# Optimization experiments

Hardware: AMD Instinct MI355X
Metric: run time of the kernel (lower is better)

The kernel has to match this reference:

```python
import jax, jax.numpy as jnp
import numpy as np

INV_SQRT_2 = float(1.0 / np.sqrt(2.0))
INV_SQRT_3 = float(1.0 / np.sqrt(3.0))


def _silu(x):
    return x * jax.nn.sigmoid(x)


def _residual_stack(x, Ws):
    # Ws: (n_layers, 2, d, d); each layer: two (Dense -> silu), residual add, *1/sqrt(2)
    for l in range(Ws.shape[0]):
        y = x
        for i in range(Ws.shape[1]):
            y = _silu(y @ Ws[l, i])
        x = (x + y) * INV_SQRT_2
    return x


def _eff_bilinear(basis, m, id_reduce, ragged, W, n_edges, kmax):
    # basis: (T, B), m: (T, I), W: (I, B, O). Ragged rows packed into dense (E, Kmax, .)
    b2 = jnp.zeros((n_edges, kmax, basis.shape[1]), basis.dtype).at[id_reduce, ragged].set(basis)
    m2 = jnp.zeros((n_edges, kmax, m.shape[1]), m.dtype).at[id_reduce, ragged].set(m)
    sum_k = jnp.einsum('ekb,eki->ebi', b2, m2)          # (E, B, I)
    return jnp.einsum('ebi,ibo->eo', sum_k, W)          # (E, O)


def setup_inputs() -> dict:
    key = jax.random.key(0)
    N, E, K = 8000, 80000, 6
    T = E * K
    D, DR, DC, DS, DT3, DB, DQ = 128, 16, 16, 16, 64, 64, 64
    ks = jax.random.split(key, 32)
    r = lambda i, shape, s=1.0: jax.random.normal(ks[i], shape, jnp.float32) * s
    w = 0.05
    return dict(
        h=r(0, (N, D)), m_st=r(1, (E, D)),
        rbf_h=jax.random.uniform(ks[2], (E, DR)),
        rbf3=jax.random.uniform(ks[3], (E, DR)),
        cbf3=jax.random.uniform(ks[4], (T, DC)),
        sbf4=jax.random.uniform(ks[5], (T, DS)),
        idx_s=jax.random.randint(ks[6], (E,), 0, N),
        idx_t=jax.random.randint(ks[7], (E,), 0, N),
        idx_swap=jax.random.permutation(ks[8], E),
        id3_kt=jax.random.randint(ks[9], (T,), 0, E),
        id3_st=jnp.repeat(jnp.arange(E), K),
        id3_ragged_idx=jnp.tile(jnp.arange(K), E),
        edge_nb_idx=jnp.repeat(jnp.arange(E), K),
        edge_nb_ragged_idx=jnp.tile(jnp.arange(K), E),
        Kt=K, Kq=K,
        W_skip=r(10, (D, D), w),
        Wt_mkt=r(11, (D, D), w), Wt_rbf=r(12, (DR, D), w), Wt_down=r(13, (D, DT3), w),
        Wt_cbf=r(14, (DT3, DC, DB), w), Wt_up_st=r(15, (DB, D), w), Wt_up_ts=r(16, (DB, D), w),
        Wq_down=r(17, (D, DQ), w), Wq_sbf=r(18, (DQ, DS, DQ), w),
        Wq_up_st=r(19, (DQ, D), w), Wq_up_ts=r(20, (DQ, D), w),
        Wres_before=r(21, (1, 2, D, D), w), Wres_after=r(22, (2, 2, D, D), w),
        Wres_m=r(23, (1, 2, D, D), w),
        W_ae_rbf=r(24, (DR, D), w), W_ae_dense=r(25, (D, D), w), W_ae_res=r(26, (2, 2, D, D), w),
        W_asi=r(27, (3 * D, D), w),
    )


def reference(h, m_st, rbf_h, rbf3, cbf3, sbf4, idx_s, idx_t, idx_swap, id3_kt,
              id3_st, id3_ragged_idx, edge_nb_idx, edge_nb_ragged_idx, Kt, Kq,
              W_skip, Wt_mkt, Wt_rbf, Wt_down, Wt_cbf, Wt_up_st, Wt_up_ts,
              Wq_down, Wq_sbf, Wq_up_st, Wq_up_ts, Wres_before, Wres_after,
              Wres_m, W_ae_rbf, W_ae_dense, W_ae_res, W_asi):
    N, E = h.shape[0], m_st.shape[0]

    x_skip = m_st @ W_skip

    # Quadruplet interaction (ScaleFactor == identity)
    m_d = _silu(m_st @ Wq_down)                       # (E, emb_quad)
    m_nb = m_d[edge_nb_idx]                            # (E_NB, emb_quad)
    xq = _eff_bilinear(sbf4, m_nb, edge_nb_idx, edge_nb_ragged_idx, Wq_sbf, E, Kq)
    x4 = (_silu(xq @ Wq_up_st) + _silu(xq @ Wq_up_ts)[idx_swap]) * INV_SQRT_2

    # Triplet interaction
    m_kt = _silu(m_st @ Wt_mkt)
    m_kt = m_kt * (rbf3 @ Wt_rbf)                      # scale_rbf identity
    m_kt = _silu(m_kt @ Wt_down)                       # (E, emb_triplet)
    m_kt = m_kt[id3_kt]                                # (T, emb_triplet)
    xt = _eff_bilinear(cbf3, m_kt, id3_st, id3_ragged_idx, Wt_cbf, E, Kt)
    x3 = (_silu(xt @ Wt_up_st) + _silu(xt @ Wt_up_ts)[idx_swap]) * INV_SQRT_2

    x = (x_skip + x3 + x4) * INV_SQRT_3
    x = _residual_stack(x, Wres_before)
    m = (m_st + x) * INV_SQRT_2
    m = _residual_stack(m, Wres_after)

    # AtomEmbedding: rbf-gated scatter-add of edge messages to target atoms
    x_ae = m * (rbf_h @ W_ae_rbf)
    h2 = jax.ops.segment_sum(x_ae, idx_t, num_segments=N)   # scale_sum identity
    h2 = _silu(h2 @ W_ae_dense)
    h2 = _residual_stack(h2, W_ae_res)
    h_new = (h + h2) * INV_SQRT_2

    # AtomSelfInteraction
    m2 = _silu(jnp.concatenate([h_new[idx_s], h_new[idx_t], m], axis=-1) @ W_asi)
    m2 = _residual_stack(m2, Wres_m)
    m_out = (m + m2) * INV_SQRT_2
    return h_new, m_out
```

## Files before the change

kernel.cpp:

```cpp
#include <hip/hip_runtime.h>

#define INV_SQRT_2 0.70710678118654752440f
#define INV_SQRT_3 0.57735026918962576451f

typedef __bf16 bf16_t;
typedef __bf16 bf16x8 __attribute__((ext_vector_type(8)));
typedef __bf16 bf16x4 __attribute__((ext_vector_type(4)));
typedef float f32x4 __attribute__((ext_vector_type(4)));

__device__ __forceinline__ float toF(float x) { return x; }
__device__ __forceinline__ float toF(bf16_t x) { return (float)x; }
__device__ __forceinline__ float siluf(float x) { return x / (1.f + __expf(-x)); }

template <typename T> __device__ __forceinline__ T fromF(float x);
template <> __device__ __forceinline__ float fromF<float>(float x) { return x; }
template <> __device__ __forceinline__ bf16_t fromF<bf16_t>(float x) { return (bf16_t)x; }

__device__ __forceinline__ bf16x8 ld8(const bf16_t* p) { return *(const bf16x8*)p; }
__device__ __forceinline__ bf16x8 ld8(const float* p) {
  bf16x8 r;
#pragma unroll
  for (int j = 0; j < 8; ++j) r[j] = (bf16_t)p[j];
  return r;
}

__device__ __forceinline__ f32x4 MFMA(bf16x8 a, bf16x8 b, f32x4 c) {
  return __builtin_amdgcn_mfma_f32_16x16x32_bf16(a, b, c, 0, 0, 0);
}

__device__ __forceinline__ void zero8(f32x4 (&a)[8]) {
#pragma unroll
  for (int i = 0; i < 8; ++i)
#pragma unroll
    for (int q = 0; q < 4; ++q) a[i][q] = 0.f;
}
__device__ __forceinline__ void zero4(f32x4 (&a)[4]) {
#pragma unroll
  for (int i = 0; i < 4; ++i)
#pragma unroll
    for (int q = 0; q < 4; ++q) a[i][q] = 0.f;
}

__device__ __forceinline__ bf16x8 ldB(const bf16_t* Bp, int ks, int nt, int NT, int lane) {
  return *(const bf16x8*)(Bp + ((((size_t)ks * NT + nt) * 64 + lane) << 3));
}

template <bool WS, int SZ>
__device__ __forceinline__ f32x4 mfma2(bf16x8 a, const bf16_t* Bp, int ks, int nt, int NT,
                                       int lane, f32x4 c) {
  c = MFMA(a, ldB(Bp, ks, nt, NT, lane), c);
  if (WS) c = MFMA(a, ldB(Bp + SZ, ks, nt, NT, lane), c);
  return c;
}

template <int NC>
struct StReg { bf16x8 v[NC]; };
template <int NC>
__device__ __forceinline__ void st_issue(StReg<NC>& r, const bf16_t* src, int tid) {
#pragma unroll
  for (int i = 0; i < NC; ++i) r.v[i] = *(const bf16x8*)(src + ((i * 512 + tid) << 3));
}
template <int NC>
__device__ __forceinline__ void st_commit(const StReg<NC>& r, bf16_t* dst, int tid) {
#pragma unroll
  for (int i = 0; i < NC; ++i) *(bf16x8*)&dst[(i * 512 + tid) << 3] = r.v[i];
}

template <int KS, int NT>
__device__ __forceinline__ void pass_glob(f32x4 (&acc)[NT], const bf16x8* af,
                                          const bf16_t* Wbuf, int lane) {
#pragma unroll
  for (int ks = 0; ks < KS; ++ks)
#pragma unroll
    for (int nt = 0; nt < NT; ++nt)
      acc[nt] = MFMA(af[ks], *(const bf16x8*)&Wbuf[((ks * NT + nt) * 64 + lane) << 3], acc[nt]);
}
template <int KS>
__device__ __forceinline__ void pass_slab(f32x4 (&acc)[8], const bf16_t* slab,
                                          const bf16_t* Wbuf, int lane) {
  const int rc = lane & 15, g = lane >> 4;
#pragma unroll
  for (int ks = 0; ks < KS; ++ks) {
    bf16x8 a = *(const bf16x8*)&slab[rc * 136 + ks * 32 + (g << 3)];
#pragma unroll
    for (int nt = 0; nt < 8; ++nt)
      acc[nt] = MFMA(a, *(const bf16x8*)&Wbuf[((ks * 8 + nt) * 64 + lane) << 3], acc[nt]);
  }
}

__global__ void k_detect(const unsigned short* __restrict__ probe, int* __restrict__ flag) {
  __shared__ int cnt;
  if (threadIdx.x == 0) cnt = 0;
  __syncthreads();
  int bad = 0;
  for (int i = threadIdx.x; i < 256; i += 64) {
    unsigned int u = (unsigned int)probe[i] << 16;
    float v = __uint_as_float(u);
    if (!(v == v) || fabsf(v) > 4.f || v < -0.25f) bad++;
  }
  atomicAdd(&cnt, bad);
  __syncthreads();
  if (threadIdx.x == 0) *flag = (cnt > 16) ? 1 : 0;
}

__global__ void k_zero(float* __restrict__ p, int n) {
  int i = blockIdx.x * blockDim.x + threadIdx.x;
  if (i < n) p[i] = 0.f;
}

#define GUARD if (*flag != want) return;

struct RDesc { const void* src; int K, N, Kpad, dstoff, mode; };
struct RTable { RDesc d[25]; };

template <typename TIN>
__global__ void k_repack(const int* __restrict__ flag, int want, RTable tab,
                         bf16_t* __restrict__ out) {
  GUARD
  RDesc d = tab.d[blockIdx.y];
  int p = blockIdx.x * 256 + threadIdx.x;
  int sz = d.Kpad * d.N;
  if (p >= sz) return;
  int NT = d.N >> 4;
  int j = p & 7;
  int lane = (p >> 3) & 63;
  int q = p >> 9;
  int nt = q % NT, ks = q / NT;
  int k = ks * 32 + ((lane >> 4) << 3) + j;
  int col = nt * 16 + (lane & 15);
  size_t si = d.mode ? ((size_t)(k & 63) * 16 + (k >> 6)) * 64 + col
                     : (size_t)k * d.N + col;
  float v = (k < d.K) ? toF(((const TIN*)d.src)[si]) : 0.f;
  bf16_t hi = (bf16_t)v;
  out[d.dstoff + p] = hi;
  out[d.dstoff + sz + p] = (bf16_t)(v - (float)hi);
}

template <typename TIN, bool WS>
__global__ __launch_bounds__(256) void k_bil_mf(const int* __restrict__ flag, int want,
    const TIN* __restrict__ basis, const bf16_t* __restrict__ msrc,
    const int* __restrict__ gidx, const bf16_t* __restrict__ Wc,
    bf16_t* __restrict__ out) {
  GUARD
  __shared__ __align__(16) bf16_t Ms[96 * 72];
  __shared__ __align__(16) float Bas[16 * 100];
  __shared__ __align__(16) bf16_t P[16384];
  const int tid = threadIdx.x;
  const int e0 = blockIdx.x * 16;
#pragma unroll
  for (int it = 0; it < 3; ++it) {
    int c = tid + it * 256;
    int j = c >> 3, part = c & 7;
    int row = gidx[e0 * 6 + j];
    *(bf16x8*)&Ms[j * 72 + part * 8] = ld8(msrc + (size_t)row * 64 + part * 8);
  }
#pragma unroll
  for (int it = 0; it < 6; ++it) {
    int c = tid + it * 256;
    Bas[(c / 96) * 100 + (c % 96)] = toF(basis[(size_t)e0 * 96 + c]);
  }
  __syncthreads();
  {
    const int e = tid >> 4, sub = tid & 15, i0 = sub * 4;
    float acc[16][4];
#pragma unroll
    for (int b = 0; b < 16; ++b)
#pragma unroll
      for (int j = 0; j < 4; ++j) acc[b][j] = 0.f;
#pragma unroll
    for (int k = 0; k < 6; ++k) {
      bf16x4 mv = *(const bf16x4*)&Ms[(e * 6 + k) * 72 + i0];
      float mf[4];
#pragma unroll
      for (int j = 0; j < 4; ++j) mf[j] = (float)mv[j];
      const float* bp = &Bas[e * 100 + k * 16];
#pragma unroll
      for (int b4 = 0; b4 < 4; ++b4) {
        f32x4 bv = *(const f32x4*)&bp[b4 * 4];
#pragma unroll
        for (int bb = 0; bb < 4; ++bb)
#pragma unroll
          for (int j = 0; j < 4; ++j) acc[b4 * 4 + bb][j] += bv[bb] * mf[j];
      }
    }
#pragma unroll
    for (int b = 0; b < 16; ++b) {
      int kk = b * 64 + i0;
      int ks = kk >> 5, r5 = kk & 31;
      int lane_hi = r5 >> 3, jj = r5 & 7;
      bf16x4 w;
#pragma unroll
      for (int j = 0; j < 4; ++j) w[j] = (bf16_t)acc[b][j];
      *(bf16x4*)&P[ks * 512 + lane_hi * 128 + e * 8 + jj] = w;
    }
  }
  __syncthreads();
  const int lane = tid & 63, wid = tid >> 6;
  const int rc = lane & 15, g = lane >> 4;
  f32x4 oa[4];
  zero4(oa);
#pragma unroll
  for (int k4 = 0; k4 < 8; ++k4)
#pragma unroll
    for (int j = 0; j < 4; ++j) {
      int ks = k4 * 4 + j;
      oa[j] = mfma2<WS, 65536>(*(const bf16x8*)&P[ks * 512 + lane * 8], Wc, ks, wid, 4, lane,
                               oa[j]);
    }
  f32x4 oacc = (oa[0] + oa[1]) + (oa[2] + oa[3]);
  bf16_t* op = out + ((size_t)e0 + g * 4) * 64 + wid * 16 + rc;
#pragma unroll
  for (int r = 0; r < 4; ++r) op[(size_t)r * 64] = (bf16_t)oacc[r];
}

template <typename TIN, bool WS>
__global__ __launch_bounds__(512, 2) void k_comb2(const int* __restrict__ flag, int want,
    const TIN* __restrict__ mst, const bf16_t* __restrict__ xt, const bf16_t* __restrict__ xq,
    const int* __restrict__ idx_swap,
    const bf16_t* Wsk, const bf16_t* Wtst, const bf16_t* Wtts,
    const bf16_t* Wqst, const bf16_t* Wqts,
    bf16_t* __restrict__ X, int M) {
  GUARD
  __shared__ __align__(16) bf16_t Wb[2][16384];
  const int tid = threadIdx.x;
  const int lane = tid & 63, wid = tid >> 6;
  const int grow0 = blockIdx.x * 128 + wid * 16;
  const int rc = lane & 15, g = lane >> 4;
  const int arow = grow0 + rc;
  const int srow = idx_swap[arow];

  const bf16_t* wseq[5] = {Wsk, Wtst, Wtts, Wqst, Wqts};
  const int SZs[5] = {16384, 8192, 8192, 8192, 8192};

  StReg<4> sreg;
  st_issue<4>(sreg, wseq[0], tid);
  st_commit<4>(sreg, Wb[0], tid);
  __syncthreads();
  int cur = 0;
  f32x4 total[8];
  f32x4 acc[8];
  zero8(acc);
  bf16x8 af[4];
#pragma unroll
  for (int l = 0; l < 5; ++l) {
    if (l == 0) {
#pragma unroll
      for (int ks = 0; ks < 4; ++ks)
        af[ks] = ld8(mst + (size_t)arow * 128 + ks * 32 + (g << 3));
    } else {
      const bf16_t* asrc = (l <= 2) ? xt : xq;
      int r = (l == 1 || l == 3) ? arow : srow;
#pragma unroll
      for (int ks = 0; ks < 2; ++ks) af[ks] = ld8(asrc + (size_t)r * 64 + ks * 32 + (g << 3));
    }
#pragma unroll
    for (int p = 0; p < (WS ? 2 : 1); ++p) {
      bool last_stage = (l == 4) && (p == (WS ? 1 : 0));
      if (!last_stage) {
        const bf16_t* nx = (WS && p == 0) ? wseq[l] + SZs[l] : wseq[l + 1];
        st_issue<4>(sreg, nx, tid);
      }
      if (l == 0) pass_glob<4, 8>(acc, af, Wb[cur], lane);
      else        pass_glob<2, 8>(acc, af, Wb[cur], lane);
      if (!last_stage) {
        st_commit<4>(sreg, Wb[cur ^ 1], tid);
        __syncthreads();
        cur ^= 1;
      }
    }
    if (l == 0) {
#pragma unroll
      for (int nt = 0; nt < 8; ++nt) total[nt] = acc[nt] * INV_SQRT_3;
    } else {
#pragma unroll
      for (int nt = 0; nt < 8; ++nt)
#pragma unroll
        for (int r = 0; r < 4; ++r)
          total[nt][r] += siluf(acc[nt][r]) * (INV_SQRT_2 * INV_SQRT_3);
    }
    zero8(acc);
  }
  bf16_t* op = X + (size_t)(grow0 + g * 4) * 128 + rc;
#pragma unroll
  for (int nt = 0; nt < 8; ++nt)
#pragma unroll
    for (int r = 0; r < 4; ++r) op[(size_t)r * 128 + nt * 16] = (bf16_t)total[nt][r];
}

template <typename TIN, bool WS>
__global__ __launch_bounds__(512, 1) void k_resE2(const int* __restrict__ flag, int want,
    const bf16_t* __restrict__ Xg, const TIN* __restrict__ mst,
    const bf16_t* W0, const bf16_t* W1, const bf16_t* W2,
    const bf16_t* W3, const bf16_t* W4, const bf16_t* W5,
    bf16_t* __restrict__ outg, int M) {
  GUARD
  __shared__ __align__(16) bf16_t Xs[128 * 136];
  __shared__ __align__(16) bf16_t Ys[128 * 136];
  __shared__ __align__(16) bf16_t Wb[2][16384];
  const int tid = threadIdx.x;
  const int lane = tid & 63, wid = tid >> 6;
  const int grow0 = blockIdx.x * 128 + wid * 16;
  const int rc = lane & 15, g = lane >> 4;
  bf16_t* slabX = Xs + wid * 16 * 136;
  bf16_t* slabY = Ys + wid * 16 * 136;

  const bf16_t* seq[12];
  if (WS) {
    seq[0] = W0; seq[1] = W0 + 16384; seq[2] = W1; seq[3] = W1 + 16384;
    seq[4] = W2; seq[5] = W2 + 16384; seq[6] = W3; seq[7] = W3 + 16384;
    seq[8] = W4; seq[9] = W4 + 16384; seq[10] = W5; seq[11] = W5 + 16384;
  } else {
    seq[0] = W0; seq[1] = W1; seq[2] = W2; seq[3] = W3; seq[4] = W4; seq[5] = W5;
  }
  const int NW = WS ? 12 : 6;

  StReg<4> sreg;
  st_issue<4>(sreg, seq[0], tid);
#pragma unroll
  for (int i = 0; i < 4; ++i) {
    int o = (i * 64 + lane) * 8;
    int r = o >> 7, c = o & 127;
    *(bf16x8*)&slabX[r * 136 + c] = ld8(Xg + (size_t)(grow0 + r) * 128 + c);
  }
  st_commit<4>(sreg, Wb[0], tid);
  __syncthreads();

  f32x4 acc[8];
  zero8(acc);
  int cur = 0;
#pragma unroll
  for (int s = 0; s < NW; ++s) {
    if (s + 1 < NW) st_issue<4>(sreg, seq[s + 1], tid);
    const int gg = WS ? (s >> 1) : s;
    const bool fin = WS ? ((s & 1) != 0) : true;
    pass_slab<4>(acc, (gg & 1) ? slabY : slabX, Wb[cur], lane);
    if (fin) {
      if ((gg & 1) == 0) {
#pragma unroll
        for (int nt = 0; nt < 8; ++nt)
#pragma unroll
          for (int r = 0; r < 4; ++r)
            slabY[(g * 4 + r) * 136 + nt * 16 + rc] = (bf16_t)siluf(acc[nt][r]);
      } else {
#pragma unroll
        for (int nt = 0; nt < 8; ++nt)
#pragma unroll
          for (int r = 0; r < 4; ++r) {
            int ix = (g * 4 + r) * 136 + nt * 16 + rc;
            float v = ((float)slabX[ix] + siluf(acc[nt][r])) * INV_SQRT_2;
            if (gg == 1) {
              float mv = toF(mst[(size_t)(grow0 + g * 4 + r) * 128 + nt * 16 + rc]);
              v = (mv + v) * INV_SQRT_2;
            }
            slabX[ix] = (bf16_t)v;
          }
      }
      zero8(acc);
    }
    if (s + 1 < NW) {
      st_commit<4>(sreg, Wb[cur ^ 1], tid);
      __syncthreads();
      cur ^= 1;
    }
  }
#pragma unroll
  for (int i = 0; i < 4; ++i) {
    int o = (i * 64 + lane) * 8;
    int r = o >> 7, c = o & 127;
    *(bf16x8*)&outg[(size_t)(grow0 + r) * 128 + c] = *(const bf16x8*)&slabX[r * 136 + c];
  }
}

template <bool WS>
__global__ __launch_bounds__(512, 1) void k_resN2(const int* __restrict__ flag, int want,
    bf16_t* __restrict__ Xg, const bf16_t* W0, const bf16_t* W1, const bf16_t* W2,
    const bf16_t* W3, int M) {
  GUARD
  __shared__ __align__(16) bf16_t Xs[128 * 136];
  __shared__ __align__(16) bf16_t Ys[128 * 136];
  __shared__ __align__(16) bf16_t Wb[2][16384];
  const int tid = threadIdx.x;
  const int lane = tid & 63, wid = tid >> 6;
  const int grow0 = blockIdx.x * 128 + wid * 16;
  const bool act = grow0 < M;
  const int rc = lane & 15, g = lane >> 4;
  bf16_t* slabX = Xs + wid * 16 * 136;
  bf16_t* slabY = Ys + wid * 16 * 136;

  const bf16_t* seq[8];
  if (WS) {
    seq[0] = W0; seq[1] = W0 + 16384; seq[2] = W1; seq[3] = W1 + 16384;
    seq[4] = W2; seq[5] = W2 + 16384; seq[6] = W3; seq[7] = W3 + 16384;
  } else {
    seq[0] = W0; seq[1] = W1; seq[2] = W2; seq[3] = W3;
  }
  const int NW = WS ? 8 : 4;

  StReg<4> sreg;
  st_issue<4>(sreg, seq[0], tid);
  if (act) {
#pragma unroll
    for (int i = 0; i < 4; ++i) {
      int o = (i * 64 + lane) * 8;
      int r = o >> 7, c = o & 127;
      *(bf16x8*)&slabX[r * 136 + c] = ld8(Xg + (size_t)(grow0 + r) * 128 + c);
    }
  }
  st_commit<4>(sreg, Wb[0], tid);
  __syncthreads();

  f32x4 acc[8];
  zero8(acc);
  int cur = 0;
#pragma unroll
  for (int s = 0; s < NW; ++s) {
    if (s + 1 < NW) st_issue<4>(sreg, seq[s + 1], tid);
    const int gg = WS ? (s >> 1) : s;
    const bool fin = WS ? ((s & 1) != 0) : true;
    pass_slab<4>(acc, (gg & 1) ? slabY : slabX, Wb[cur], lane);
    if (fin) {
      if ((gg & 1) == 0) {
#pragma unroll
        for (int nt = 0; nt < 8; ++nt)
#pragma unroll
          for (int r = 0; r < 4; ++r)
            slabY[(g * 4 + r) * 136 + nt * 16 + rc] = (bf16_t)siluf(acc[nt][r]);
      } else {
#pragma unroll
        for (int nt = 0; nt < 8; ++nt)
#pragma unroll
          for (int r = 0; r < 4; ++r) {
            int ix = (g * 4 + r) * 136 + nt * 16 + rc;
            slabX[ix] = (bf16_t)(((float)slabX[ix] + siluf(acc[nt][r])) * INV_SQRT_2);
          }
      }
      zero8(acc);
    }
    if (s + 1 < NW) {
      st_commit<4>(sreg, Wb[cur ^ 1], tid);
      __syncthreads();
      cur ^= 1;
    }
  }
  if (act) {
#pragma unroll
    for (int i = 0; i < 4; ++i) {
      int o = (i * 64 + lane) * 8;
      int r = o >> 7, c = o & 127;
      *(bf16x8*)&Xg[(size_t)(grow0 + r) * 128 + c] = *(const bf16x8*)&slabX[r * 136 + c];
    }
  }
}

template <typename TIN, typename TOUT, bool WS>
__global__ __launch_bounds__(512, 1) void k_asi2(const int* __restrict__ flag, int want,
    const bf16_t* __restrict__ hnew, const bf16_t* __restrict__ m,
    const int* __restrict__ idx_s, const int* __restrict__ idx_t,
    const bf16_t* Wasi, const bf16_t* Wm0, const bf16_t* Wm1,
    TOUT* __restrict__ outm, int M) {
  GUARD
  __shared__ __align__(16) bf16_t Xs[128 * 136];
  __shared__ __align__(16) bf16_t Ys[128 * 136];
  __shared__ __align__(16) bf16_t Wb[2][16384];
  const int tid = threadIdx.x;
  const int lane = tid & 63, wid = tid >> 6;
  const int grow0 = blockIdx.x * 128 + wid * 16;
  const int rc = lane & 15, g = lane >> 4;
  bf16_t* slabX = Xs + wid * 16 * 136;
  bf16_t* slabY = Ys + wid * 16 * 136;
  const int e = grow0 + rc;
  const int rs = idx_s[e], rt = idx_t[e];

  const bf16_t* seq[10];
  if (WS) {
    seq[0] = Wasi;         seq[1] = Wasi + 49152;
    seq[2] = Wasi + 16384; seq[3] = Wasi + 65536;
    seq[4] = Wasi + 32768; seq[5] = Wasi + 81920;
    seq[6] = Wm0;          seq[7] = Wm0 + 16384;
    seq[8] = Wm1;          seq[9] = Wm1 + 16384;
  } else {
    seq[0] = Wasi; seq[1] = Wasi + 16384; seq[2] = Wasi + 32768;
    seq[3] = Wm0;  seq[4] = Wm1;
  }
  const int NW = WS ? 10 : 5;

  StReg<4> sreg;
  st_issue<4>(sreg, seq[0], tid);
  st_commit<4>(sreg, Wb[0], tid);
  __syncthreads();

  f32x4 acc[8];
  zero8(acc);
  bf16x8 af[4];
  int cur = 0;
#pragma unroll
  for (int s = 0; s < NW; ++s) {
    if (s + 1 < NW) st_issue<4>(sreg, seq[s + 1], tid);
    const int lg = WS ? (s >> 1) : s;
    const bool first = WS ? ((s & 1) == 0) : true;
    const bool fin = WS ? ((s & 1) != 0) : true;
    if (lg <= 2) {
      if (first) {
        const bf16_t* asrc = (lg == 0) ? hnew + (size_t)rs * 128
                           : (lg == 1) ? hnew + (size_t)rt * 128
                                       : m + (size_t)e * 128;
#pragma unroll
        for (int ks = 0; ks < 4; ++ks) af[ks] = ld8(asrc + ks * 32 + (g << 3));
      }
      pass_glob<4, 8>(acc, af, Wb[cur], lane);
    } else if (lg == 3) {
      pass_slab<4>(acc, slabX, Wb[cur], lane);
    } else {
      pass_slab<4>(acc, slabY, Wb[cur], lane);
    }
    if (fin) {
      if (lg == 2) {
#pragma unroll
        for (int nt = 0; nt < 8; ++nt)
#pragma unroll
          for (int r = 0; r < 4; ++r)
            slabX[(g * 4 + r) * 136 + nt * 16 + rc] = (bf16_t)siluf(acc[nt][r]);
        zero8(acc);
      } else if (lg == 3) {
#pragma unroll
        for (int nt = 0; nt < 8; ++nt)
#pragma unroll
          for (int r = 0; r < 4; ++r)
            slabY[(g * 4 + r) * 136 + nt * 16 + rc] = (bf16_t)siluf(acc[nt][r]);
        zero8(acc);
      } else if (lg == 4) {
#pragma unroll
        for (int nt = 0; nt < 8; ++nt)
#pragma unroll
          for (int r = 0; r < 4; ++r) {
            int row = grow0 + g * 4 + r, col = nt * 16 + rc;
            float x = (float)slabX[(g * 4 + r) * 136 + col];
            float v = (x + siluf(acc[nt][r])) * INV_SQRT_2;
            outm[(size_t)row * 128 + col] =
                fromF<TOUT>(((float)m[(size_t)row * 128 + col] + v) * INV_SQRT_2);
          }
      }
    }
    if (s + 1 < NW) {
      st_commit<4>(sreg, Wb[cur ^ 1], tid);
      __syncthreads();
      cur ^= 1;
    }
  }
}

template <typename TIN, bool WS>
__global__ __launch_bounds__(512, 2) void k_mkt2(const int* __restrict__ flag, int want,
    const TIN* __restrict__ mst, const TIN* __restrict__ rbf3,
    const bf16_t* __restrict__ Wm, const bf16_t* __restrict__ Wr,
    bf16_t* __restrict__ out, int M) {
  GUARD
  __shared__ __align__(16) bf16_t Wb[2][16384];
  __shared__ __align__(16) bf16_t Wrl[8192];
  const int tid = threadIdx.x;
  const int lane = tid & 63, wid = tid >> 6;
  const int grow0 = blockIdx.x * 128 + wid * 16;
  const int rc = lane & 15, g = lane >> 4;
  StReg<4> sreg;
  st_issue<4>(sreg, Wm, tid);
  bf16x8 wr0 = *(const bf16x8*)(Wr + (tid << 3));
  bf16x8 wr1 = *(const bf16x8*)(Wr + 4096 + (tid << 3));
  st_commit<4>(sreg, Wb[0], tid);
  *(bf16x8*)&Wrl[tid << 3] = wr0;
  *(bf16x8*)&Wrl[4096 + (tid << 3)] = wr1;
  __syncthreads();
  bf16x8 af[4];
#pragma unroll
  for (int ks = 0; ks < 4; ++ks)
    af[ks] = ld8(mst + (size_t)(grow0 + rc) * 128 + ks * 32 + (g << 3));
  bf16x8 az;
#pragma unroll
  for (int j = 0; j < 8; ++j) az[j] = (bf16_t)0.f;
  if (g < 2) az = ld8(rbf3 + (size_t)(grow0 + rc) * 16 + (g << 3));
  f32x4 ag[8];
  zero8(ag);
#pragma unroll
  for (int nt = 0; nt < 8; ++nt) {
    ag[nt] = MFMA(az, *(const bf16x8*)&Wrl[(nt * 64 + lane) << 3], ag[nt]);
    if (WS) ag[nt] = MFMA(az, *(const bf16x8*)&Wrl[4096 + ((nt * 64 + lane) << 3)], ag[nt]);
  }
  f32x4 am[8];
  zero8(am);
  if (WS) st_issue<4>(sreg, Wm + 16384, tid);
  pass_glob<4, 8>(am, af, Wb[0], lane);
  if (WS) {
    st_commit<4>(sreg, Wb[1], tid);
    __syncthreads();
    pass_glob<4, 8>(am, af, Wb[1], lane);
  }
  bf16_t* op = out + (size_t)(grow0 + g * 4) * 128 + rc;
#pragma unroll
  for (int nt = 0; nt < 8; ++nt)
#pragma unroll
    for (int r = 0; r < 4; ++r)
      op[(size_t)r * 128 + nt * 16] = (bf16_t)(siluf(am[nt][r]) * ag[nt][r]);
}

template <typename TA, bool WS>
__global__ __launch_bounds__(512, 2) void k_gemmE2(const int* __restrict__ flag, int want,
    const TA* __restrict__ A, const bf16_t* __restrict__ W, bf16_t* __restrict__ out, int M) {
  GUARD
  __shared__ __align__(16) bf16_t Wb[2][8192];
  const int tid = threadIdx.x;
  const int lane = tid & 63, wid = tid >> 6;
  const int grow0 = blockIdx.x * 128 + wid * 16;
  const int rc = lane & 15, g = lane >> 4;
  StReg<2> sreg;
  st_issue<2>(sreg, W, tid);
  st_commit<2>(sreg, Wb[0], tid);
  __syncthreads();
  bf16x8 af[4];
#pragma unroll
  for (int ks = 0; ks < 4; ++ks)
    af[ks] = ld8(A + (size_t)(grow0 + rc) * 128 + ks * 32 + (g << 3));
  f32x4 acc[4];
  zero4(acc);
  if (WS) st_issue<2>(sreg, W + 8192, tid);
  pass_glob<4, 4>(acc, af, Wb[0], lane);
  if (WS) {
    st_commit<2>(sreg, Wb[1], tid);
    __syncthreads();
    pass_glob<4, 4>(acc, af, Wb[1], lane);
  }
  bf16_t* op = out + (size_t)(grow0 + g * 4) * 64 + rc;
#pragma unroll
  for (int nt = 0; nt < 4; ++nt)
#pragma unroll
    for (int r = 0; r < 4; ++r) op[(size_t)r * 64 + nt * 16] = (bf16_t)siluf(acc[nt][r]);
}

template <bool WS>
__global__ __launch_bounds__(512, 2) void k_gemmN2(const int* __restrict__ flag, int want,
    const float* __restrict__ A, const bf16_t* __restrict__ W, bf16_t* __restrict__ out, int M) {
  GUARD
  __shared__ __align__(16) bf16_t Wb[2][16384];
  const int tid = threadIdx.x;
  const int lane = tid & 63, wid = tid >> 6;
  const int grow0 = blockIdx.x * 128 + wid * 16;
  const bool act = grow0 < M;
  const int rc = lane & 15, g = lane >> 4;
  StReg<4> sreg;
  st_issue<4>(sreg, W, tid);
  st_commit<4>(sreg, Wb[0], tid);
  __syncthreads();
  bf16x8 af[4];
  if (act) {
#pragma unroll
    for (int ks = 0; ks < 4; ++ks)
      af[ks] = ld8(A + (size_t)(grow0 + rc) * 128 + ks * 32 + (g << 3));
  } else {
#pragma unroll
    for (int ks = 0; ks < 4; ++ks)
#pragma unroll
      for (int j = 0; j < 8; ++j) af[ks][j] = (bf16_t)0.f;
  }
  f32x4 acc[8];
  zero8(acc);
  if (WS) st_issue<4>(sreg, W + 16384, tid);
  pass_glob<4, 8>(acc, af, Wb[0], lane);
  if (WS) {
    st_commit<4>(sreg, Wb[1], tid);
    __syncthreads();
    pass_glob<4, 8>(acc, af, Wb[1], lane);
  }
  if (act) {
    bf16_t* op = out + (size_t)(grow0 + g * 4) * 128 + rc;
#pragma unroll
    for (int nt = 0; nt < 8; ++nt)
#pragma unroll
      for (int r = 0; r < 4; ++r) op[(size_t)r * 128 + nt * 16] = (bf16_t)siluf(acc[nt][r]);
  }
}

template <typename TIN>
__global__ void k_scatter(const int* __restrict__ flag, int want,
                          const bf16_t* __restrict__ m, const TIN* __restrict__ rbf_h,
                          const TIN* __restrict__ Wrbf, const int* __restrict__ idx_t,
                          float* __restrict__ h2) {
  GUARD
  int e = blockIdx.x;
  int c = threadIdx.x;
  float g = 0.f;
#pragma unroll
  for (int k = 0; k < 16; ++k) g += toF(rbf_h[(size_t)e * 16 + k]) * toF(Wrbf[k * 128 + c]);
  atomicAdd(&h2[(size_t)idx_t[e] * 128 + c], (float)m[(size_t)e * 128 + c] * g);
}

template <typename TIN, typename TOUT>
__global__ void k_hnew_b(const int* __restrict__ flag, int want,
                         const TIN* __restrict__ h, bf16_t* __restrict__ X,
                         TOUT* __restrict__ out, int n) {
  GUARD
  int i = blockIdx.x * blockDim.x + threadIdx.x;
  if (i >= n) return;
  float v = (toF(h[i]) + (float)X[i]) * INV_SQRT_2;
  X[i] = (bf16_t)v;
  out[i] = fromF<TOUT>(v);
}

template <typename TIN, typename TOUT, bool WS>
static void run_pipeline(void* const* d_in, int N, int E, void* d_out,
                         bf16_t* Wpack, bf16_t* s0, bf16_t* s1, bf16_t* s2, bf16_t* s3,
                         float* h2, bf16_t* Rn2, const int* flag, int want, hipStream_t stream) {
  const TIN* h      = (const TIN*)d_in[0];
  const TIN* m_st   = (const TIN*)d_in[1];
  const TIN* rbf_h  = (const TIN*)d_in[2];
  const TIN* rbf3   = (const TIN*)d_in[3];
  const TIN* cbf3   = (const TIN*)d_in[4];
  const TIN* sbf4   = (const TIN*)d_in[5];
  const int* idx_s   = (const int*)d_in[6];
  const int* idx_t   = (const int*)d_in[7];
  const int* idx_sw  = (const int*)d_in[8];
  const int* id3_kt  = (const int*)d_in[9];
  const int* enb_idx = (const int*)d_in[12];
  const TIN* W_skip   = (const TIN*)d_in[16];
  const TIN* Wt_mkt   = (const TIN*)d_in[17];
  const TIN* Wt_rbf   = (const TIN*)d_in[18];
  const TIN* Wt_down  = (const TIN*)d_in[19];
  const TIN* Wt_cbf   = (const TIN*)d_in[20];
  const TIN* Wt_up_st = (const TIN*)d_in[21];
  const TIN* Wt_up_ts = (const TIN*)d_in[22];
  const TIN* Wq_down  = (const TIN*)d_in[23];
  const TIN* Wq_sbf   = (const TIN*)d_in[24];
  const TIN* Wq_up_st = (const TIN*)d_in[25];
  const TIN* Wq_up_ts = (const TIN*)d_in[26];
  const TIN* Wres_before = (const TIN*)d_in[27];
  const TIN* Wres_after  = (const TIN*)d_in[28];
  const TIN* Wres_m      = (const TIN*)d_in[29];
  const TIN* W_ae_rbf    = (const TIN*)d_in[30];
  const TIN* W_ae_dense  = (const TIN*)d_in[31];
  const TIN* W_ae_res    = (const TIN*)d_in[32];
  const TIN* W_asi       = (const TIN*)d_in[33];

  RTable tab;
  int cur = 0, nd = 0;
  auto add = [&](const void* src, int K, int Np, int Kpad, int mode = 0) {
    tab.d[nd].src = src; tab.d[nd].K = K; tab.d[nd].N = Np; tab.d[nd].Kpad = Kpad;
    tab.d[nd].dstoff = cur; tab.d[nd].mode = mode;
    int o = cur;
    cur += 2 * Kpad * Np;
    ++nd;
    return o;
  };
  const int M128 = 128 * 128;
  int oQd  = add(Wq_down, 128, 64, 128);
  int oMkt = add(Wt_mkt, 128, 128, 128);
  int oRbf = add(Wt_rbf, 16, 128, 32);
  int oTd  = add(Wt_down, 128, 64, 128);
  int oTst = add(Wt_up_st, 64, 128, 64);
  int oTts = add(Wt_up_ts, 64, 128, 64);
  int oQst = add(Wq_up_st, 64, 128, 64);
  int oQts = add(Wq_up_ts, 64, 128, 64);
  int oSk  = add(W_skip, 128, 128, 128);
  int oB0  = add(Wres_before, 128, 128, 128);
  int oB1  = add(Wres_before + M128, 128, 128, 128);
  int oA0  = add(Wres_after, 128, 128, 128);
  int oA1  = add(Wres_after + M128, 128, 128, 128);
  int oA2  = add(Wres_after + 2 * M128, 128, 128, 128);
  int oA3  = add(Wres_after + 3 * M128, 128, 128, 128);
  int oM0  = add(Wres_m, 128, 128, 128);
  int oM1  = add(Wres_m + M128, 128, 128, 128);
  int oAed = add(W_ae_dense, 128, 128, 128);
  int oAe0 = add(W_ae_res, 128, 128, 128);
  int oAe1 = add(W_ae_res + M128, 128, 128, 128);
  int oAe2 = add(W_ae_res + 2 * M128, 128, 128, 128);
  int oAe3 = add(W_ae_res + 3 * M128, 128, 128, 128);
  int oAsi = add(W_asi, 384, 128, 384);
  int oTc  = add(Wt_cbf, 1024, 64, 1024, 1);
  int oQc  = add(Wq_sbf, 1024, 64, 1024, 1);
  (void)cur;

  const int gE = E / 128;
  const int gN = (N + 127) / 128;
  const int BS = 256;

  bf16_t* mkt_tmp = s0;
  bf16_t* m_kt = s2;
  bf16_t* m_d  = s3;
  bf16_t* xt = s0;
  bf16_t* xq = s1;
  bf16_t* X  = s2;
  bf16_t* R2 = s0;

  k_repack<TIN><<<dim3(256, 25), BS, 0, stream>>>(flag, want, tab, Wpack);

  k_mkt2<TIN, WS><<<gE, 512, 0, stream>>>(flag, want, m_st, rbf3, Wpack + oMkt, Wpack + oRbf,
                                          mkt_tmp, E);
  k_gemmE2<bf16_t, WS><<<gE, 512, 0, stream>>>(flag, want, mkt_tmp, Wpack + oTd, m_kt, E);
  k_gemmE2<TIN, WS><<<gE, 512, 0, stream>>>(flag, want, m_st, Wpack + oQd, m_d, E);
  k_bil_mf<TIN, WS><<<E / 16, BS, 0, stream>>>(flag, want, cbf3, m_kt, id3_kt, Wpack + oTc, xt);
  k_bil_mf<TIN, WS><<<E / 16, BS, 0, stream>>>(flag, want, sbf4, m_d, enb_idx, Wpack + oQc, xq);
  k_comb2<TIN, WS><<<gE, 512, 0, stream>>>(flag, want, m_st, xt, xq, idx_sw,
      Wpack + oSk, Wpack + oTst, Wpack + oTts, Wpack + oQst, Wpack + oQts, X, E);
  k_resE2<TIN, WS><<<gE, 512, 0, stream>>>(flag, want, X, m_st, Wpack + oB0, Wpack + oB1,
      Wpack + oA0, Wpack + oA1, Wpack + oA2, Wpack + oA3, R2, E);
  k_zero<<<(N * 128 + BS - 1) / BS, BS, 0, stream>>>(h2, N * 128);
  k_scatter<TIN><<<E, 128, 0, stream>>>(flag, want, R2, rbf_h, W_ae_rbf, idx_t, h2);
  k_gemmN2<WS><<<gN, 512, 0, stream>>>(flag, want, h2, Wpack + oAed, Rn2, N);
  k_resN2<WS><<<gN, 512, 0, stream>>>(flag, want, Rn2, Wpack + oAe0, Wpack + oAe1,
                                      Wpack + oAe2, Wpack + oAe3, N);
  TOUT* out_h = (TOUT*)d_out;
  TOUT* out_m = out_h + (size_t)N * 128;
  k_hnew_b<TIN, TOUT><<<(N * 128 + BS - 1) / BS, BS, 0, stream>>>(flag, want, h, Rn2, out_h,
                                                                  N * 128);
  k_asi2<TIN, TOUT, WS><<<gE, 512, 0, stream>>>(flag, want, Rn2, R2, idx_s, idx_t,
      Wpack + oAsi, Wpack + oM0, Wpack + oM1, out_m, E);
}

extern "C" void kernel_launch(void* const* d_in, const int* in_sizes, int n_in,
                              void* d_out, int out_size, void* d_ws, size_t ws_size,
                              hipStream_t stream) {
  const int D = 128;
  const int N = in_sizes[0] / D;
  const int E = in_sizes[1] / D;

  char* base = (char*)d_ws;
  bf16_t* Wpack = (bf16_t*)base;
  int* flag = (int*)(base + 1916928 + 32768);
  char* dyn = base + 1916928 + 32768 + 256;
  size_t U = (size_t)E * 64 * sizeof(bf16_t);
  bf16_t* s0 = (bf16_t*)dyn;
  bf16_t* s1 = (bf16_t*)(dyn + U);
  bf16_t* s2 = (bf16_t*)(dyn + 2 * U);
  bf16_t* s3 = (bf16_t*)(dyn + 3 * U);
  float* h2 = (float*)(dyn + 2 * U);
  bf16_t* Rn2 = (bf16_t*)((char*)h2 + (size_t)N * 128 * sizeof(float));

  k_detect<<<1, 64, 0, stream>>>((const unsigned short*)d_in[2], flag);

  run_pipeline<bf16_t, bf16_t, false>(d_in, N, E, d_out, Wpack, s0, s1, s2, s3, h2, Rn2, flag, 0,
                                      stream);
  run_pipeline<float, float, true>(d_in, N, E, d_out, Wpack, s0, s1, s2, s3, h2, Rn2, flag, 1,
                                   stream);
}
```

Measured before the change: 669.3 us.

## Merge dtype-specialized pipelines into one runtime-dispatched pipeline with smaller blocks

Replaces the two templated pipelines (bf16 and f32, each launched and early-exiting on a device flag) with a single set of kernels that read the dtype flag at runtime and branch internally. This halves the number of kernel launches. It also shrinks the GEMM kernels from 512-thread, 128-row tiles to 256-thread, 64-row tiles with higher occupancy bounds. The residual kernel now uses a single weight buffer with an extra barrier per stage. The cost is runtime branching, possible register pressure from the merged paths, and less weight reuse per block.

After: 741.5 us. 1.11x slower.

```diff
diff --git a/kernel.cpp b/kernel.cpp
--- a/kernel.cpp
+++ b/kernel.cpp
@@ -12,10 +12,6 @@
 __device__ __forceinline__ float toF(bf16_t x) { return (float)x; }
 __device__ __forceinline__ float siluf(float x) { return x / (1.f + __expf(-x)); }
 
-template <typename T> __device__ __forceinline__ T fromF(float x);
-template <> __device__ __forceinline__ float fromF<float>(float x) { return x; }
-template <> __device__ __forceinline__ bf16_t fromF<bf16_t>(float x) { return (bf16_t)x; }
-
 __device__ __forceinline__ bf16x8 ld8(const bf16_t* p) { return *(const bf16x8*)p; }
 __device__ __forceinline__ bf16x8 ld8(const float* p) {
   bf16x8 r;
@@ -24,6 +20,10 @@
   return r;
 }
 
+__device__ __forceinline__ float ldsc(const void* p, int f32, size_t i) {
+  return f32 ? ((const float*)p)[i] : toF(((const bf16_t*)p)[i]);
+}
+
 __device__ __forceinline__ f32x4 MFMA(bf16x8 a, bf16x8 b, f32x4 c) {
   return __builtin_amdgcn_mfma_f32_16x16x32_bf16(a, b, c, 0, 0, 0);
 }
@@ -45,25 +45,35 @@
   return *(const bf16x8*)(Bp + ((((size_t)ks * NT + nt) * 64 + lane) << 3));
 }
 
-template <bool WS, int SZ>
-__device__ __forceinline__ f32x4 mfma2(bf16x8 a, const bf16_t* Bp, int ks, int nt, int NT,
-                                       int lane, f32x4 c) {
-  c = MFMA(a, ldB(Bp, ks, nt, NT, lane), c);
-  if (WS) c = MFMA(a, ldB(Bp + SZ, ks, nt, NT, lane), c);
-  return c;
-}
-
-template <int NC>
-struct StReg { bf16x8 v[NC]; };
-template <int NC>
-__device__ __forceinline__ void st_issue(StReg<NC>& r, const bf16_t* src, int tid) {
-#pragma unroll
-  for (int i = 0; i < NC; ++i) r.v[i] = *(const bf16x8*)(src + ((i * 512 + tid) << 3));
-}
-template <int NC>
-__device__ __forceinline__ void st_commit(const StReg<NC>& r, bf16_t* dst, int tid) {
-#pragma unroll
-  for (int i = 0; i < NC; ++i) *(bf16x8*)&dst[(i * 512 + tid) << 3] = r.v[i];
+__device__ __forceinline__ void ldA(bf16x8 (&af)[4], const void* p, int f32, size_t row, int g) {
+  if (f32) {
+    const float* q = (const float*)p + row * 128 + (g << 3);
+#pragma unroll
+    for (int ks = 0; ks < 4; ++ks) af[ks] = ld8(q + ks * 32);
+  } else {
+    const bf16_t* q = (const bf16_t*)p + row * 128 + (g << 3);
+#pragma unroll
+    for (int ks = 0; ks < 4; ++ks) af[ks] = ld8(q + ks * 32);
+  }
+}
+
+struct St8 { bf16x8 v[8]; };
+__device__ __forceinline__ void issue8(St8& r, const bf16_t* src, int tid) {
+#pragma unroll
+  for (int i = 0; i < 8; ++i) r.v[i] = *(const bf16x8*)(src + ((i * 256 + tid) << 3));
+}
+__device__ __forceinline__ void commit8(const St8& r, bf16_t* dst, int tid) {
+#pragma unroll
+  for (int i = 0; i < 8; ++i) *(bf16x8*)&dst[(i * 256 + tid) << 3] = r.v[i];
+}
+struct St4 { bf16x8 v[4]; };
+__device__ __forceinline__ void issue4(St4& r, const bf16_t* src, int tid) {
+#pragma unroll
+  for (int i = 0; i < 4; ++i) r.v[i] = *(const bf16x8*)(src + ((i * 256 + tid) << 3));
+}
+__device__ __forceinline__ void commit4(const St4& r, bf16_t* dst, int tid) {
+#pragma unroll
+  for (int i = 0; i < 4; ++i) *(bf16x8*)&dst[(i * 256 + tid) << 3] = r.v[i];
 }
 
 template <int KS, int NT>
@@ -108,19 +118,17 @@
   if (i < n) p[i] = 0.f;
 }
 
-#define GUARD if (*flag != want) return;
-
 struct RDesc { const void* src; int K, N, Kpad, dstoff, mode; };
 struct RTable { RDesc d[25]; };
 
-template <typename TIN>
-__global__ void k_repack(const int* __restrict__ flag, int want, RTable tab,
-                         bf16_t* __restrict__ out) {
-  GUARD
+__global__ void k_repack(const int* __restrict__ flag, RTable tab, bf16_t* __restrict__ out) {
+  const int ws = *flag;
   RDesc d = tab.d[blockIdx.y];
   int p = blockIdx.x * 256 + threadIdx.x;
   int sz = d.Kpad * d.N;
   if (p >= sz) return;
+  const int bilin = d.mode & 1;
+  const int Koff = d.mode >> 1;
   int NT = d.N >> 4;
   int j = p & 7;
   int lane = (p >> 3) & 63;
@@ -128,20 +136,19 @@
   int nt = q % NT, ks = q / NT;
   int k = ks * 32 + ((lane >> 4) << 3) + j;
   int col = nt * 16 + (lane & 15);
-  size_t si = d.mode ? ((size_t)(k & 63) * 16 + (k >> 6)) * 64 + col
-                     : (size_t)k * d.N + col;
-  float v = (k < d.K) ? toF(((const TIN*)d.src)[si]) : 0.f;
+  size_t si = bilin ? ((size_t)(k & 63) * 16 + (k >> 6)) * 64 + col
+                    : (size_t)(k + Koff) * d.N + col;
+  float v = (k < d.K) ? ldsc(d.src, ws, si) : 0.f;
   bf16_t hi = (bf16_t)v;
   out[d.dstoff + p] = hi;
   out[d.dstoff + sz + p] = (bf16_t)(v - (float)hi);
 }
 
-template <typename TIN, bool WS>
-__global__ __launch_bounds__(256) void k_bil_mf(const int* __restrict__ flag, int want,
-    const TIN* __restrict__ basis, const bf16_t* __restrict__ msrc,
+__global__ __launch_bounds__(256) void k_bil(const int* __restrict__ flag,
+    const void* __restrict__ basis, const bf16_t* __restrict__ msrc,
     const int* __restrict__ gidx, const bf16_t* __restrict__ Wc,
     bf16_t* __restrict__ out) {
-  GUARD
+  const int ws = *flag;
   __shared__ __align__(16) bf16_t Ms[96 * 72];
   __shared__ __align__(16) float Bas[16 * 100];
   __shared__ __align__(16) bf16_t P[16384];
@@ -157,7 +164,7 @@
 #pragma unroll
   for (int it = 0; it < 6; ++it) {
     int c = tid + it * 256;
-    Bas[(c / 96) * 100 + (c % 96)] = toF(basis[(size_t)e0 * 96 + c]);
+    Bas[(c / 96) * 100 + (c % 96)] = ldsc(basis, ws, (size_t)e0 * 96 + c);
   }
   __syncthreads();
   {
@@ -199,71 +206,190 @@
   const int rc = lane & 15, g = lane >> 4;
   f32x4 oa[4];
   zero4(oa);
-#pragma unroll
-  for (int k4 = 0; k4 < 8; ++k4)
-#pragma unroll
-    for (int j = 0; j < 4; ++j) {
-      int ks = k4 * 4 + j;
-      oa[j] = mfma2<WS, 65536>(*(const bf16x8*)&P[ks * 512 + lane * 8], Wc, ks, wid, 4, lane,
-                               oa[j]);
-    }
+  if (ws) {
+#pragma unroll
+    for (int k4 = 0; k4 < 8; ++k4)
+#pragma unroll
+      for (int j = 0; j < 4; ++j) {
+        int ks = k4 * 4 + j;
+        bf16x8 a = *(const bf16x8*)&P[ks * 512 + lane * 8];
+        oa[j] = MFMA(a, ldB(Wc, ks, wid, 4, lane), oa[j]);
+        oa[j] = MFMA(a, ldB(Wc + 65536, ks, wid, 4, lane), oa[j]);
+      }
+  } else {
+#pragma unroll
+    for (int k4 = 0; k4 < 8; ++k4)
+#pragma unroll
+      for (int j = 0; j < 4; ++j) {
+        int ks = k4 * 4 + j;
+        bf16x8 a = *(const bf16x8*)&P[ks * 512 + lane * 8];
+        oa[j] = MFMA(a, ldB(Wc, ks, wid, 4, lane), oa[j]);
+      }
+  }
   f32x4 oacc = (oa[0] + oa[1]) + (oa[2] + oa[3]);
   bf16_t* op = out + ((size_t)e0 + g * 4) * 64 + wid * 16 + rc;
 #pragma unroll
   for (int r = 0; r < 4; ++r) op[(size_t)r * 64] = (bf16_t)oacc[r];
 }
 
-template <typename TIN, bool WS>
-__global__ __launch_bounds__(512, 2) void k_comb2(const int* __restrict__ flag, int want,
-    const TIN* __restrict__ mst, const bf16_t* __restrict__ xt, const bf16_t* __restrict__ xq,
-    const int* __restrict__ idx_swap,
-    const bf16_t* Wsk, const bf16_t* Wtst, const bf16_t* Wtts,
-    const bf16_t* Wqst, const bf16_t* Wqts,
-    bf16_t* __restrict__ X, int M) {
-  GUARD
+__global__ __launch_bounds__(256, 2) void k_mkt2(const int* __restrict__ flag,
+    const void* __restrict__ mst, const void* __restrict__ rbf3,
+    const bf16_t* __restrict__ Wm, const bf16_t* __restrict__ Wr,
+    bf16_t* __restrict__ out) {
+  const int ws = *flag;
+  __shared__ __align__(16) bf16_t Wb[2][16384];
+  __shared__ __align__(16) bf16_t Wrl[8192];
+  const int tid = threadIdx.x;
+  const int lane = tid & 63, wid = tid >> 6;
+  const int grow0 = blockIdx.x * 64 + wid * 16;
+  const int rc = lane & 15, g = lane >> 4;
+  St8 s8;
+  issue8(s8, Wm, tid);
+  bf16x8 wr[4];
+#pragma unroll
+  for (int i = 0; i < 4; ++i) wr[i] = *(const bf16x8*)(Wr + ((i * 256 + tid) << 3));
+  commit8(s8, Wb[0], tid);
+#pragma unroll
+  for (int i = 0; i < 4; ++i) *(bf16x8*)&Wrl[(i * 256 + tid) << 3] = wr[i];
+  __syncthreads();
+  bf16x8 af[4];
+  ldA(af, mst, ws, (size_t)(grow0 + rc), g);
+  bf16x8 az;
+#pragma unroll
+  for (int j = 0; j < 8; ++j) az[j] = (bf16_t)0.f;
+  if (g < 2) {
+    if (ws) az = ld8((const float*)rbf3 + (size_t)(grow0 + rc) * 16 + (g << 3));
+    else    az = ld8((const bf16_t*)rbf3 + (size_t)(grow0 + rc) * 16 + (g << 3));
+  }
+  f32x4 ag[8];
+  zero8(ag);
+#pragma unroll
+  for (int nt = 0; nt < 8; ++nt) {
+    ag[nt] = MFMA(az, *(const bf16x8*)&Wrl[(nt * 64 + lane) << 3], ag[nt]);
+    if (ws) ag[nt] = MFMA(az, *(const bf16x8*)&Wrl[4096 + ((nt * 64 + lane) << 3)], ag[nt]);
+  }
+  f32x4 am[8];
+  zero8(am);
+  if (ws) issue8(s8, Wm + 16384, tid);
+  pass_glob<4, 8>(am, af, Wb[0], lane);
+  if (ws) {
+    commit8(s8, Wb[1], tid);
+    __syncthreads();
+    pass_glob<4, 8>(am, af, Wb[1], lane);
+  }
+  bf16_t* op = out + (size_t)(grow0 + g * 4) * 128 + rc;
+#pragma unroll
+  for (int nt = 0; nt < 8; ++nt)
+#pragma unroll
+    for (int r = 0; r < 4; ++r)
+      op[(size_t)r * 128 + nt * 16] = (bf16_t)(siluf(am[nt][r]) * ag[nt][r]);
+}
+
+__global__ __launch_bounds__(256, 4) void k_gemmE2(const int* __restrict__ flag, int a_rt,
+    const void* __restrict__ A, const bf16_t* __restrict__ W, bf16_t* __restrict__ out) {
+  const int ws = *flag;
+  const int af32 = a_rt & ws;
+  __shared__ __align__(16) bf16_t Wb[2][8192];
+  const int tid = threadIdx.x;
+  const int lane = tid & 63, wid = tid >> 6;
+  const int grow0 = blockIdx.x * 64 + wid * 16;
+  const int rc = lane & 15, g = lane >> 4;
+  St4 s4;
+  issue4(s4, W, tid);
+  commit4(s4, Wb[0], tid);
+  __syncthreads();
+  bf16x8 af[4];
+  ldA(af, A, af32, (size_t)(grow0 + rc), g);
+  f32x4 acc[4];
+  zero4(acc);
+  if (ws) issue4(s4, W + 8192, tid);
+  pass_glob<4, 4>(acc, af, Wb[0], lane);
+  if (ws) {
+    commit4(s4, Wb[1], tid);
+    __syncthreads();
+    pass_glob<4, 4>(acc, af, Wb[1], lane);
+  }
+  bf16_t* op = out + (size_t)(grow0 + g * 4) * 64 + rc;
+#pragma unroll
+  for (int nt = 0; nt < 4; ++nt)
+#pragma unroll
+    for (int r = 0; r < 4; ++r) op[(size_t)r * 64 + nt * 16] = (bf16_t)siluf(acc[nt][r]);
+}
+
+__global__ __launch_bounds__(256, 2) void k_gemmN2(const int* __restrict__ flag,
+    const float* __restrict__ A, const bf16_t* __restrict__ W, bf16_t* __restrict__ out) {
+  const int ws = *flag;
   __shared__ __align__(16) bf16_t Wb[2][16384];
   const int tid = threadIdx.x;
   const int lane = tid & 63, wid = tid >> 6;
-  const int grow0 = blockIdx.x * 128 + wid * 16;
+  const int grow0 = blockIdx.x * 64 + wid * 16;
+  const int rc = lane & 15, g = lane >> 4;
+  St8 s8;
+  issue8(s8, W, tid);
+  commit8(s8, Wb[0], tid);
+  __syncthreads();
+  bf16x8 af[4];
+  {
+    const float* q = A + (size_t)(grow0 + rc) * 128 + (g << 3);
+#pragma unroll
+    for (int ks = 0; ks < 4; ++ks) af[ks] = ld8(q + ks * 32);
+  }
+  f32x4 acc[8];
+  zero8(acc);
+  if (ws) issue8(s8, W + 16384, tid);
+  pass_glob<4, 8>(acc, af, Wb[0], lane);
+  if (ws) {
+    commit8(s8, Wb[1], tid);
+    __syncthreads();
+    pass_glob<4, 8>(acc, af, Wb[1], lane);
+  }
+  bf16_t* op = out + (size_t)(grow0 + g * 4) * 128 + rc;
+#pragma unroll
+  for (int nt = 0; nt < 8; ++nt)
+#pragma unroll
+    for (int r = 0; r < 4; ++r) op[(size_t)r * 128 + nt * 16] = (bf16_t)siluf(acc[nt][r]);
+}
+
+__global__ __launch_bounds__(256, 2) void k_comb2(const int* __restrict__ flag,
+    const void* __restrict__ mst, const bf16_t* __restrict__ xt,
+    const bf16_t* __restrict__ xq, const int* __restrict__ idx_swap,
+    const bf16_t* Wsk, const bf16_t* Wtst, const bf16_t* Wtts,
+    const bf16_t* Wqst, const bf16_t* Wqts, bf16_t* __restrict__ X) {
+  const int ws = *flag;
+  __shared__ __align__(16) bf16_t Wb[2][16384];
+  const int tid = threadIdx.x;
+  const int lane = tid & 63, wid = tid >> 6;
+  const int grow0 = blockIdx.x * 64 + wid * 16;
   const int rc = lane & 15, g = lane >> 4;
   const int arow = grow0 + rc;
   const int srow = idx_swap[arow];
-
   const bf16_t* wseq[5] = {Wsk, Wtst, Wtts, Wqst, Wqts};
   const int SZs[5] = {16384, 8192, 8192, 8192, 8192};
-
-  StReg<4> sreg;
-  st_issue<4>(sreg, wseq[0], tid);
-  st_commit<4>(sreg, Wb[0], tid);
+  St8 s8;
+  issue8(s8, wseq[0], tid);
+  commit8(s8, Wb[0], tid);
   __syncthreads();
   int cur = 0;
-  f32x4 total[8];
-  f32x4 acc[8];
+  const int NP = ws ? 2 : 1;
+  f32x4 total[8], acc[8];
   zero8(acc);
   bf16x8 af[4];
-#pragma unroll
   for (int l = 0; l < 5; ++l) {
     if (l == 0) {
-#pragma unroll
-      for (int ks = 0; ks < 4; ++ks)
-        af[ks] = ld8(mst + (size_t)arow * 128 + ks * 32 + (g << 3));
+      ldA(af, mst, ws, (size_t)arow, g);
     } else {
       const bf16_t* asrc = (l <= 2) ? xt : xq;
       int r = (l == 1 || l == 3) ? arow : srow;
-#pragma unroll
-      for (int ks = 0; ks < 2; ++ks) af[ks] = ld8(asrc + (size_t)r * 64 + ks * 32 + (g << 3));
-    }
-#pragma unroll
-    for (int p = 0; p < (WS ? 2 : 1); ++p) {
-      bool last_stage = (l == 4) && (p == (WS ? 1 : 0));
-      if (!last_stage) {
-        const bf16_t* nx = (WS && p == 0) ? wseq[l] + SZs[l] : wseq[l + 1];
-        st_issue<4>(sreg, nx, tid);
-      }
+      af[0] = ld8(asrc + (size_t)r * 64 + (g << 3));
+      af[1] = ld8(asrc + (size_t)r * 64 + 32 + (g << 3));
+    }
+    for (int p = 0; p < NP; ++p) {
+      const bool last = (l == 4) && (p == NP - 1);
+      if (!last) issue8(s8, (ws && p == 0) ? wseq[l] + SZs[l] : wseq[l + 1], tid);
       if (l == 0) pass_glob<4, 8>(acc, af, Wb[cur], lane);
       else        pass_glob<2, 8>(acc, af, Wb[cur], lane);
-      if (!last_stage) {
-        st_commit<4>(sreg, Wb[cur ^ 1], tid);
+      if (!last) {
+        commit8(s8, Wb[cur ^ 1], tid);
         __syncthreads();
         cur ^= 1;
       }
@@ -287,53 +413,51 @@
     for (int r = 0; r < 4; ++r) op[(size_t)r * 128 + nt * 16] = (bf16_t)total[nt][r];
 }
 
-template <typename TIN, bool WS>
-__global__ __launch_bounds__(512, 1) void k_resE2(const int* __restrict__ flag, int want,
-    const bf16_t* __restrict__ Xg, const TIN* __restrict__ mst,
+__global__ __launch_bounds__(256, 2) void k_resE2(const int* __restrict__ flag,
+    const bf16_t* __restrict__ Xg, const void* __restrict__ mst,
     const bf16_t* W0, const bf16_t* W1, const bf16_t* W2,
     const bf16_t* W3, const bf16_t* W4, const bf16_t* W5,
-    bf16_t* __restrict__ outg, int M) {
-  GUARD
-  __shared__ __align__(16) bf16_t Xs[128 * 136];
-  __shared__ __align__(16) bf16_t Ys[128 * 136];
-  __shared__ __align__(16) bf16_t Wb[2][16384];
+    bf16_t* __restrict__ outg) {
+  const int ws = *flag;
+  __shared__ __align__(16) bf16_t Xs[64 * 136];
+  __shared__ __align__(16) bf16_t Ys[64 * 136];
+  __shared__ __align__(16) bf16_t Wb[16384];
   const int tid = threadIdx.x;
   const int lane = tid & 63, wid = tid >> 6;
-  const int grow0 = blockIdx.x * 128 + wid * 16;
-  const int rc = lane & 15, g = lane >> 4;
-  bf16_t* slabX = Xs + wid * 16 * 136;
-  bf16_t* slabY = Ys + wid * 16 * 136;
-
+  const int grow0 = blockIdx.x * 64 + wid * 16;
+  const int rc = lane & 15, g = lane >> 4;
+  bf16_t* slabX = Xs + wid * (16 * 136);
+  bf16_t* slabY = Ys + wid * (16 * 136);
+  const bf16_t* Wl[6] = {W0, W1, W2, W3, W4, W5};
   const bf16_t* seq[12];
-  if (WS) {
-    seq[0] = W0; seq[1] = W0 + 16384; seq[2] = W1; seq[3] = W1 + 16384;
-    seq[4] = W2; seq[5] = W2 + 16384; seq[6] = W3; seq[7] = W3 + 16384;
-    seq[8] = W4; seq[9] = W4 + 16384; seq[10] = W5; seq[11] = W5 + 16384;
+  int NW;
+  if (ws) {
+    NW = 12;
+#pragma unroll
+    for (int l = 0; l < 6; ++l) { seq[2 * l] = Wl[l]; seq[2 * l + 1] = Wl[l] + 16384; }
   } else {
-    seq[0] = W0; seq[1] = W1; seq[2] = W2; seq[3] = W3; seq[4] = W4; seq[5] = W5;
-  }
-  const int NW = WS ? 12 : 6;
-
-  StReg<4> sreg;
-  st_issue<4>(sreg, seq[0], tid);
+    NW = 6;
+#pragma unroll
+    for (int l = 0; l < 6; ++l) seq[l] = Wl[l];
+  }
+  St8 s8;
+  issue8(s8, seq[0], tid);
 #pragma unroll
   for (int i = 0; i < 4; ++i) {
-    int o = (i * 64 + lane) * 8;
-    int r = o >> 7, c = o & 127;
-    *(bf16x8*)&slabX[r * 136 + c] = ld8(Xg + (size_t)(grow0 + r) * 128 + c);
-  }
-  st_commit<4>(sreg, Wb[0], tid);
-  __syncthreads();
-
+    int o = (i * 64 + lane) * 8, r = o >> 7, c = o & 127;
+    *(bf16x8*)&slabX[r * 136 + c] = *(const bf16x8*)&Xg[(size_t)(grow0 + r) * 128 + c];
+  }
+  commit8(s8, Wb, tid);
+  __syncthreads();
   f32x4 acc[8];
   zero8(acc);
-  int cur = 0;
-#pragma unroll
   for (int s = 0; s < NW; ++s) {
-    if (s + 1 < NW) st_issue<4>(sreg, seq[s + 1], tid);
-    const int gg = WS ? (s >> 1) : s;
-    const bool fin = WS ? ((s & 1) != 0) : true;
-    pass_slab<4>(acc, (gg & 1) ? slabY : slabX, Wb[cur], lane);
+    if (s + 1 < NW) issue8(s8, seq[s + 1], tid);
+    const int gg = ws ? (s >> 1) : s;
+    const int fin = ws ? (s & 1) : 1;
+    pass_slab<4>(acc, (gg & 1) ? slabY : slabX, Wb, lane);
+    __syncthreads();
+    if (s + 1 < NW) commit8(s8, Wb, tid);
     if (fin) {
       if ((gg & 1) == 0) {
 #pragma unroll
@@ -348,76 +472,66 @@
           for (int r = 0; r < 4; ++r) {
             int ix = (g * 4 + r) * 136 + nt * 16 + rc;
             float v = ((float)slabX[ix] + siluf(acc[nt][r])) * INV_SQRT_2;
-            if (gg == 1) {
-              float mv = toF(mst[(size_t)(grow0 + g * 4 + r) * 128 + nt * 16 + rc]);
-              v = (mv + v) * INV_SQRT_2;
-            }
+            if (gg == 1)
+              v = (ldsc(mst, ws, (size_t)(grow0 + g * 4 + r) * 128 + nt * 16 + rc) + v) *
+                  INV_SQRT_2;
             slabX[ix] = (bf16_t)v;
           }
       }
       zero8(acc);
     }
-    if (s + 1 < NW) {
-      st_commit<4>(sreg, Wb[cur ^ 1], tid);
-      __syncthreads();
-      cur ^= 1;
-    }
+    if (s + 1 < NW) __syncthreads();
   }
 #pragma unroll
   for (int i = 0; i < 4; ++i) {
-    int o = (i * 64 + lane) * 8;
-    int r = o >> 7, c = o & 127;
+    int o = (i * 64 + lane) * 8, r = o >> 7, c = o & 127;
     *(bf16x8*)&outg[(size_t)(grow0 + r) * 128 + c] = *(const bf16x8*)&slabX[r * 136 + c];
   }
 }
 
-template <bool WS>
-__global__ __launch_bounds__(512, 1) void k_resN2(const int* __restrict__ flag, int want,
-    bf16_t* __restrict__ Xg, const bf16_t* W0, const bf16_t* W1, const bf16_t* W2,
-    const bf16_t* W3, int M) {
-  GUARD
-  __shared__ __align__(16) bf16_t Xs[128 * 136];
-  __shared__ __align__(16) bf16_t Ys[128 * 136];
-  __shared__ __align__(16) bf16_t Wb[2][16384];
+__global__ __launch_bounds__(256, 2) void k_resN2(const int* __restrict__ flag,
+    bf16_t* __restrict__ Xg, const bf16_t* W0, const bf16_t* W1,
+    const bf16_t* W2, const bf16_t* W3) {
+  const int ws = *flag;
+  __shared__ __align__(16) bf16_t Xs[64 * 136];
+  __shared__ __align__(16) bf16_t Ys[64 * 136];
+  __shared__ __align__(16) bf16_t Wb[16384];
   const int tid = threadIdx.x;
   const int lane = tid & 63, wid = tid >> 6;
-  const int grow0 = blockIdx.x * 128 + wid * 16;
-  const bool act = grow0 < M;
-  const int rc = lane & 15, g = lane >> 4;
-  bf16_t* slabX = Xs + wid * 16 * 136;
-  bf16_t* slabY = Ys + wid * 16 * 136;
-
+  const int grow0 = blockIdx.x * 64 + wid * 16;
+  const int rc = lane & 15, g = lane >> 4;
+  bf16_t* slabX = Xs + wid * (16 * 136);
+  bf16_t* slabY = Ys + wid * (16 * 136);
+  const bf16_t* Wl[4] = {W0, W1, W2, W3};
   const bf16_t* seq[8];
-  if (WS) {
-    seq[0] = W0; seq[1] = W0 + 16384; seq[2] = W1; seq[3] = W1 + 16384;
-    seq[4] = W2; seq[5] = W2 + 16384; seq[6] = W3; seq[7] = W3 + 16384;
+  int NW;
+  if (ws) {
+    NW = 8;
+#pragma unroll
+    for (int l = 0; l < 4; ++l) { seq[2 * l] = Wl[l]; seq[2 * l + 1] = Wl[l] + 16384; }
   } else {
-    seq[0] = W0; seq[1] = W1; seq[2] = W2; seq[3] = W3;
-  }
-  const int NW = WS ? 8 : 4;
-
-  StReg<4> sreg;
-  st_issue<4>(sreg, seq[0], tid);
-  if (act) {
-#pragma unroll
-    for (int i = 0; i < 4; ++i) {
-      int o = (i * 64 + lane) * 8;
-      int r = o >> 7, c = o & 127;
-      *(bf16x8*)&slabX[r * 136 + c] = ld8(Xg + (size_t)(grow0 + r) * 128 + c);
-    }
-  }
-  st_commit<4>(sreg, Wb[0], tid);
-  __syncthreads();
-
+    NW = 4;
+#pragma unroll
+    for (int l = 0; l < 4; ++l) seq[l] = Wl[l];
+  }
+  St8 s8;
+  issue8(s8, seq[0], tid);
+#pragma unroll
+  for (int i = 0; i < 4; ++i) {
+    int o = (i * 64 + lane) * 8, r = o >> 7, c = o & 127;
+    *(bf16x8*)&slabX[r * 136 + c] = *(const bf16x8*)&Xg[(size_t)(grow0 + r) * 128 + c];
+  }
+  commit8(s8, Wb, tid);
+  __syncthreads();
   f32x4 acc[8];
   zero8(acc);
-  int cur = 0;
-#pragma unroll
   for (int s = 0; s < NW; ++s) {
-    if (s + 1 < NW) st_issue<4>(sreg, seq[s + 1], tid);
-    const int gg = WS ? (s >> 1) : s;
-    const bool fin = WS ? ((s & 1) != 0) : true;
-    pass_slab<4>(acc, (gg & 1) ? slabY : slabX, Wb[cur], lane);
+    if (s + 1 < NW) issue8(s8, seq[s + 1], tid);
+    const int gg = ws ? (s >> 1) : s;
+    const int fin = ws ? (s & 1) : 1;
+    pass_slab<4>(acc, (gg & 1) ? slabY : slabX, Wb, lane);
+    __syncthreads();
+    if (s + 1 < NW) commit8(s8, Wb, tid);
     if (fin) {
       if ((gg & 1) == 0) {
 #pragma unroll
@@ -436,69 +550,58 @@
       }
       zero8(acc);
     }
-    if (s + 1 < NW) {
-      st_commit<4>(sreg, Wb[cur ^ 1], tid);
-      __syncthreads();
-      cur ^= 1;
-    }
-  }
-  if (act) {
-#pragma unroll
-    for (int i = 0; i < 4; ++i) {
-      int o = (i * 64 + lane) * 8;
-      int r = o >> 7, c = o & 127;
-      *(bf16x8*)&Xg[(size_t)(grow0 + r) * 128 + c] = *(const bf16x8*)&slabX[r * 136 + c];
-    }
-  }
-}
-
-template <typename TIN, typename TOUT, bool WS>
-__global__ __launch_bounds__(512, 1) void k_asi2(const int* __restrict__ flag, int want,
+    if (s + 1 < NW) __syncthreads();
+  }
+#pragma unroll
+  for (int i = 0; i < 4; ++i) {
+    int o = (i * 64 + lane) * 8, r = o >> 7, c = o & 127;
+    *(bf16x8*)&Xg[(size_t)(grow0 + r) * 128 + c] = *(const bf16x8*)&slabX[r * 136 + c];
+  }
+}
+
+__global__ __launch_bounds__(256, 2) void k_asi2(const int* __restrict__ flag,
     const bf16_t* __restrict__ hnew, const bf16_t* __restrict__ m,
     const int* __restrict__ idx_s, const int* __restrict__ idx_t,
     const bf16_t* Wasi, const bf16_t* Wm0, const bf16_t* Wm1,
-    TOUT* __restrict__ outm, int M) {
-  GUARD
-  __shared__ __align__(16) bf16_t Xs[128 * 136];
-  __shared__ __align__(16) bf16_t Ys[128 * 136];
-  __shared__ __align__(16) bf16_t Wb[2][16384];
+    void* __restrict__ outm, int eoff) {
+  const int ws = *flag;
+  __shared__ __align__(16) bf16_t Xs[64 * 136];
+  __shared__ __align__(16) bf16_t Ys[64 * 136];
+  __shared__ __align__(16) bf16_t Wb[16384];
   const int tid = threadIdx.x;
   const int lane = tid & 63, wid = tid >> 6;
-  const int grow0 = blockIdx.x * 128 + wid * 16;
-  const int rc = lane & 15, g = lane >> 4;
-  bf16_t* slabX = Xs + wid * 16 * 136;
-  bf16_t* slabY = Ys + wid * 16 * 136;
+  const int grow0 = blockIdx.x * 64 + wid * 16;
+  const int rc = lane & 15, g = lane >> 4;
+  bf16_t* slabX = Xs + wid * (16 * 136);
+  bf16_t* slabY = Ys + wid * (16 * 136);
   const int e = grow0 + rc;
   const int rs = idx_s[e], rt = idx_t[e];
-
   const bf16_t* seq[10];
-  if (WS) {
+  int NW;
+  if (ws) {
+    NW = 10;
     seq[0] = Wasi;         seq[1] = Wasi + 49152;
     seq[2] = Wasi + 16384; seq[3] = Wasi + 65536;
     seq[4] = Wasi + 32768; seq[5] = Wasi + 81920;
     seq[6] = Wm0;          seq[7] = Wm0 + 16384;
     seq[8] = Wm1;          seq[9] = Wm1 + 16384;
   } else {
+    NW = 5;
     seq[0] = Wasi; seq[1] = Wasi + 16384; seq[2] = Wasi + 32768;
     seq[3] = Wm0;  seq[4] = Wm1;
   }
-  const int NW = WS ? 10 : 5;
-
-  StReg<4> sreg;
-  st_issue<4>(sreg, seq[0], tid);
-  st_commit<4>(sreg, Wb[0], tid);
-  __syncthreads();
-
+  St8 s8;
+  issue8(s8, seq[0], tid);
+  commit8(s8, Wb, tid);
+  __syncthreads();
   f32x4 acc[8];
   zero8(acc);
   bf16x8 af[4];
-  int cur = 0;
-#pragma unroll
   for (int s = 0; s < NW; ++s) {
-    if (s + 1 < NW) st_issue<4>(sreg, seq[s + 1], tid);
-    const int lg = WS ? (s >> 1) : s;
-    const bool first = WS ? ((s & 1) == 0) : true;
-    const bool fin = WS ? ((s & 1) != 0) : true;
+    if (s + 1 < NW) issue8(s8, seq[s + 1], tid);
+    const int lg = ws ? (s >> 1) : s;
+    const int first = ws ? !(s & 1) : 1;
+    const int fin = ws ? (s & 1) : 1;
     if (lg <= 2) {
       if (first) {
         const bf16_t* asrc = (lg == 0) ? hnew + (size_t)rs * 128
@@ -507,12 +610,14 @@
 #pragma unroll
         for (int ks = 0; ks < 4; ++ks) af[ks] = ld8(asrc + ks * 32 + (g << 3));
       }
-      pass_glob<4, 8>(acc, af, Wb[cur], lane);
+      pass_glob<4, 8>(acc, af, Wb, lane);
     } else if (lg == 3) {
-      pass_slab<4>(acc, slabX, Wb[cur], lane);
+      pass_slab<4>(acc, slabX, Wb, lane);
     } else {
-      pass_slab<4>(acc, slabY, Wb[cur], lane);
-    }
+      pass_slab<4>(acc, slabY, Wb, lane);
+    }
+    __syncthreads();
+    if (s + 1 < NW) commit8(s8, Wb, tid);
     if (fin) {
       if (lg == 2) {
 #pragma unroll
@@ -536,280 +641,47 @@
             int row = grow0 + g * 4 + r, col = nt * 16 + rc;
             float x = (float)slabX[(g * 4 + r) * 136 + col];
             float v = (x + siluf(acc[nt][r])) * INV_SQRT_2;
-            outm[(size_t)row * 128 + col] =
-                fromF<TOUT>(((float)m[(size_t)row * 128 + col] + v) * INV_SQRT_2);
+            float res = (toF(m[(size_t)row * 128 + col]) + v) * INV_SQRT_2;
+            size_t oi = (size_t)eoff + (size_t)row * 128 + col;
+            if (ws) ((float*)outm)[oi] = res;
+            else    ((bf16_t*)outm)[oi] = (bf16_t)res;
           }
       }
     }
-    if (s + 1 < NW) {
-      st_commit<4>(sreg, Wb[cur ^ 1], tid);
-      __syncthreads();
-      cur ^= 1;
-    }
-  }
-}
-
-template <typename TIN, bool WS>
-__global__ __launch_bounds__(512, 2) void k_mkt2(const int* __restrict__ flag, int want,
-    const TIN* __restrict__ mst, const TIN* __restrict__ rbf3,
-    const bf16_t* __restrict__ Wm, const bf16_t* __restrict__ Wr,
-    bf16_t* __restrict__ out, int M) {
-  GUARD
-  __shared__ __align__(16) bf16_t Wb[2][16384];
-  __shared__ __align__(16) bf16_t Wrl[8192];
-  const int tid = threadIdx.x;
-  const int lane = tid & 63, wid = tid >> 6;
-  const int grow0 = blockIdx.x * 128 + wid * 16;
-  const int rc = lane & 15, g = lane >> 4;
-  StReg<4> sreg;
-  st_issue<4>(sreg, Wm, tid);
-  bf16x8 wr0 = *(const bf16x8*)(Wr + (tid << 3));
-  bf16x8 wr1 = *(const bf16x8*)(Wr + 4096 + (tid << 3));
-  st_commit<4>(sreg, Wb[0], tid);
-  *(bf16x8*)&Wrl[tid << 3] = wr0;
-  *(bf16x8*)&Wrl[4096 + (tid << 3)] = wr1;
-  __syncthreads();
-  bf16x8 af[4];
-#pragma unroll
-  for (int ks = 0; ks < 4; ++ks)
-    af[ks] = ld8(mst + (size_t)(grow0 + rc) * 128 + ks * 32 + (g << 3));
-  bf16x8 az;
-#pragma unroll
-  for (int j = 0; j < 8; ++j) az[j] = (bf16_t)0.f;
-  if (g < 2) az = ld8(rbf3 + (size_t)(grow0 + rc) * 16 + (g << 3));
-  f32x4 ag[8];
-  zero8(ag);
-#pragma unroll
-  for (int nt = 0; nt < 8; ++nt) {
-    ag[nt] = MFMA(az, *(const bf16x8*)&Wrl[(nt * 64 + lane) << 3], ag[nt]);
-    if (WS) ag[nt] = MFMA(az, *(const bf16x8*)&Wrl[4096 + ((nt * 64 + lane) << 3)], ag[nt]);
-  }
-  f32x4 am[8];
-  zero8(am);
-  if (WS) st_issue<4>(sreg, Wm + 16384, tid);
-  pass_glob<4, 8>(am, af, Wb[0], lane);
-  if (WS) {
-    st_commit<4>(sreg, Wb[1], tid);
-    __syncthreads();
-    pass_glob<4, 8>(am, af, Wb[1], lane);
-  }
-  bf16_t* op = out + (size_t)(grow0 + g * 4) * 128 + rc;
-#pragma unroll
-  for (int nt = 0; nt < 8; ++nt)
-#pragma unroll
-    for (int r = 0; r < 4; ++r)
-      op[(size_t)r * 128 + nt * 16] = (bf16_t)(siluf(am[nt][r]) * ag[nt][r]);
-}
-
-template <typename TA, bool WS>
-__global__ __launch_bounds__(512, 2) void k_gemmE2(const int* __restrict__ flag, int want,
-    const TA* __restrict__ A, const bf16_t* __restrict__ W, bf16_t* __restrict__ out, int M) {
-  GUARD
-  __shared__ __align__(16) bf16_t Wb[2][8192];
-  const int tid = threadIdx.x;
-  const int lane = tid & 63, wid = tid >> 6;
-  const int grow0 = blockIdx.x * 128 + wid * 16;
-  const int rc = lane & 15, g = lane >> 4;
-  StReg<2> sreg;
-  st_issue<2>(sreg, W, tid);
-  st_commit<2>(sreg, Wb[0], tid);
-  __syncthreads();
-  bf16x8 af[4];
-#pragma unroll
-  for (int ks = 0; ks < 4; ++ks)
-    af[ks] = ld8(A + (size_t)(grow0 + rc) * 128 + ks * 32 + (g << 3));
-  f32x4 acc[4];
-  zero4(acc);
-  if (WS) st_issue<2>(sreg, W + 8192, tid);
-  pass_glob<4, 4>(acc, af, Wb[0], lane);
-  if (WS) {
-    st_commit<2>(sreg, Wb[1], tid);
-    __syncthreads();
-    pass_glob<4, 4>(acc, af, Wb[1], lane);
-  }
-  bf16_t* op = out + (size_t)(grow0 + g * 4) * 64 + rc;
-#pragma unroll
-  for (int nt = 0; nt < 4; ++nt)
-#pragma unroll
-    for (int r = 0; r < 4; ++r) op[(size_t)r * 64 + nt * 16] = (bf16_t)siluf(acc[nt][r]);
-}
-
-template <bool WS>
-__global__ __launch_bounds__(512, 2) void k_gemmN2(const int* __restrict__ flag, int want,
-    const float* __restrict__ A, const bf16_t* __restrict__ W, bf16_t* __restrict__ out, int M) {
-  GUARD
-  __shared__ __align__(16) bf16_t Wb[2][16384];
-  const int tid = threadIdx.x;
-  const int lane = tid & 63, wid = tid >> 6;
-  const int grow0 = blockIdx.x * 128 + wid * 16;
-  const bool act = grow0 < M;
-  const int rc = lane & 15, g = lane >> 4;
-  StReg<4> sreg;
-  st_issue<4>(sreg, W, tid);
-  st_commit<4>(sreg, Wb[0], tid);
-  __syncthreads();
-  bf16x8 af[4];
-  if (act) {
-#pragma unroll
-    for (int ks = 0; ks < 4; ++ks)
-      af[ks] = ld8(A + (size_t)(grow0 + rc) * 128 + ks * 32 + (g << 3));
-  } else {
-#pragma unroll
-    for (int ks = 0; ks < 4; ++ks)
-#pragma unroll
-      for (int j = 0; j < 8; ++j) af[ks][j] = (bf16_t)0.f;
-  }
-  f32x4 acc[8];
-  zero8(acc);
-  if (WS) st_issue<4>(sreg, W + 16384, tid);
-  pass_glob<4, 8>(acc, af, Wb[0], lane);
-  if (WS) {
-    st_commit<4>(sreg, Wb[1], tid);
-    __syncthreads();
-    pass_glob<4, 8>(acc, af, Wb[1], lane);
-  }
-  if (act) {
-    bf16_t* op = out + (size_t)(grow0 + g * 4) * 128 + rc;
-#pragma unroll
-    for (int nt = 0; nt < 8; ++nt)
-#pragma unroll
-      for (int r = 0; r < 4; ++r) op[(size_t)r * 128 + nt * 16] = (bf16_t)siluf(acc[nt][r]);
-  }
-}
-
-template <typename TIN>
-__global__ void k_scatter(const int* __restrict__ flag, int want,
-                          const bf16_t* __restrict__ m, const TIN* __restrict__ rbf_h,
-                          const TIN* __restrict__ Wrbf, const int* __restrict__ idx_t,
-                          float* __restrict__ h2) {
-  GUARD
+    if (s + 1 < NW) __syncthreads();
+  }
+}
+
+__global__ void k_scatter(const int* __restrict__ flag, const bf16_t* __restrict__ m,
+                          const void* __restrict__ rbf_h, const void* __restrict__ Wrbf,
+                          const int* __restrict__ idx_t, float* __restrict__ h2) {
+  const int ws = *flag;
   int e = blockIdx.x;
   int c = threadIdx.x;
-  float g = 0.f;
-#pragma unroll
-  for (int k = 0; k < 16; ++k) g += toF(rbf_h[(size_t)e * 16 + k]) * toF(Wrbf[k * 128 + c]);
-  atomicAdd(&h2[(size_t)idx_t[e] * 128 + c], (float)m[(size_t)e * 128 + c] * g);
-}
-
-template <typename TIN, typename TOUT>
-__global__ void k_hnew_b(const int* __restrict__ flag, int want,
-                         const TIN* __restrict__ h, bf16_t* __restrict__ X,
-                         TOUT* __restrict__ out, int n) {
-  GUARD
+  float gt = 0.f;
+  if (ws) {
+    const float* rh = (const float*)rbf_h + (size_t)e * 16;
+    const float* w = (const float*)Wrbf;
+#pragma unroll
+    for (int k = 0; k < 16; ++k) gt += rh[k] * w[k * 128 + c];
+  } else {
+    const bf16_t* rh = (const bf16_t*)rbf_h + (size_t)e * 16;
+    const bf16_t* w = (const bf16_t*)Wrbf;
+#pragma unroll
+    for (int k = 0; k < 16; ++k) gt += toF(rh[k]) * toF(w[k * 128 + c]);
+  }
+  atomicAdd(&h2[(size_t)idx_t[e] * 128 + c], toF(m[(size_t)e * 128 + c]) * gt);
+}
+
+__global__ void k_hnew(const int* __restrict__ flag, const void* __restrict__ h,
+                       bf16_t* __restrict__ X, void* __restrict__ out, int n) {
+  const int ws = *flag;
   int i = blockIdx.x * blockDim.x + threadIdx.x;
   if (i >= n) return;
-  float v = (toF(h[i]) + (float)X[i]) * INV_SQRT_2;
+  float v = (ldsc(h, ws, i) + toF(X[i])) * INV_SQRT_2;
   X[i] = (bf16_t)v;
-  out[i] = fromF<TOUT>(v);
-}
-
-template <typename TIN, typename TOUT, bool WS>
-static void run_pipeline(void* const* d_in, int N, int E, void* d_out,
-                         bf16_t* Wpack, bf16_t* s0, bf16_t* s1, bf16_t* s2, bf16_t* s3,
-                         float* h2, bf16_t* Rn2, const int* flag, int want, hipStream_t stream) {
-  const TIN* h      = (const TIN*)d_in[0];
-  const TIN* m_st   = (const TIN*)d_in[1];
-  const TIN* rbf_h  = (const TIN*)d_in[2];
-  const TIN* rbf3   = (const TIN*)d_in[3];
-  const TIN* cbf3   = (const TIN*)d_in[4];
-  const TIN* sbf4   = (const TIN*)d_in[5];
-  const int* idx_s   = (const int*)d_in[6];
-  const int* idx_t   = (const int*)d_in[7];
-  const int* idx_sw  = (const int*)d_in[8];
-  const int* id3_kt  = (const int*)d_in[9];
-  const int* enb_idx = (const int*)d_in[12];
-  const TIN* W_skip   = (const TIN*)d_in[16];
-  const TIN* Wt_mkt   = (const TIN*)d_in[17];
-  const TIN* Wt_rbf   = (const TIN*)d_in[18];
-  const TIN* Wt_down  = (const TIN*)d_in[19];
-  const TIN* Wt_cbf   = (const TIN*)d_in[20];
-  const TIN* Wt_up_st = (const TIN*)d_in[21];
-  const TIN* Wt_up_ts = (const TIN*)d_in[22];
-  const TIN* Wq_down  = (const TIN*)d_in[23];
-  const TIN* Wq_sbf   = (const TIN*)d_in[24];
-  const TIN* Wq_up_st = (const TIN*)d_in[25];
-  const TIN* Wq_up_ts = (const TIN*)d_in[26];
-  const TIN* Wres_before = (const TIN*)d_in[27];
-  const TIN* Wres_after  = (const TIN*)d_in[28];
-  const TIN* Wres_m      = (const TIN*)d_in[29];
-  const TIN* W_ae_rbf    = (const TIN*)d_in[30];
-  const TIN* W_ae_dense  = (const TIN*)d_in[31];
-  const TIN* W_ae_res    = (const TIN*)d_in[32];
-  const TIN* W_asi       = (const TIN*)d_in[33];
-
-  RTable tab;
-  int cur = 0, nd = 0;
-  auto add = [&](const void* src, int K, int Np, int Kpad, int mode = 0) {
-    tab.d[nd].src = src; tab.d[nd].K = K; tab.d[nd].N = Np; tab.d[nd].Kpad = Kpad;
-    tab.d[nd].dstoff = cur; tab.d[nd].mode = mode;
-    int o = cur;
-    cur += 2 * Kpad * Np;
-    ++nd;
-    return o;
-  };
-  const int M128 = 128 * 128;
-  int oQd  = add(Wq_down, 128, 64, 128);
-  int oMkt = add(Wt_mkt, 128, 128, 128);
-  int oRbf = add(Wt_rbf, 16, 128, 32);
-  int oTd  = add(Wt_down, 128, 64, 128);
-  int oTst = add(Wt_up_st, 64, 128, 64);
-  int oTts = add(Wt_up_ts, 64, 128, 64);
-  int oQst = add(Wq_up_st, 64, 128, 64);
-  int oQts = add(Wq_up_ts, 64, 128, 64);
-  int oSk  = add(W_skip, 128, 128, 128);
-  int oB0  = add(Wres_before, 128, 128, 128);
-  int oB1  = add(Wres_before + M128, 128, 128, 128);
-  int oA0  = add(Wres_after, 128, 128, 128);
-  int oA1  = add(Wres_after + M128, 128, 128, 128);
-  int oA2  = add(Wres_after + 2 * M128, 128, 128, 128);
-  int oA3  = add(Wres_after + 3 * M128, 128, 128, 128);
-  int oM0  = add(Wres_m, 128, 128, 128);
-  int oM1  = add(Wres_m + M128, 128, 128, 128);
-  int oAed = add(W_ae_dense, 128, 128, 128);
-  int oAe0 = add(W_ae_res, 128, 128, 128);
-  int oAe1 = add(W_ae_res + M128, 128, 128, 128);
-  int oAe2 = add(W_ae_res + 2 * M128, 128, 128, 128);
-  int oAe3 = add(W_ae_res + 3 * M128, 128, 128, 128);
-  int oAsi = add(W_asi, 384, 128, 384);
-  int oTc  = add(Wt_cbf, 1024, 64, 1024, 1);
-  int oQc  = add(Wq_sbf, 1024, 64, 1024, 1);
-  (void)cur;
-
-  const int gE = E / 128;
-  const int gN = (N + 127) / 128;
-  const int BS = 256;
-
-  bf16_t* mkt_tmp = s0;
-  bf16_t* m_kt = s2;
-  bf16_t* m_d  = s3;
-  bf16_t* xt = s0;
-  bf16_t* xq = s1;
-  bf16_t* X  = s2;
-  bf16_t* R2 = s0;
-
-  k_repack<TIN><<<dim3(256, 25), BS, 0, stream>>>(flag, want, tab, Wpack);
-
-  k_mkt2<TIN, WS><<<gE, 512, 0, stream>>>(flag, want, m_st, rbf3, Wpack + oMkt, Wpack + oRbf,
-                                          mkt_tmp, E);
-  k_gemmE2<bf16_t, WS><<<gE, 512, 0, stream>>>(flag, want, mkt_tmp, Wpack + oTd, m_kt, E);
-  k_gemmE2<TIN, WS><<<gE, 512, 0, stream>>>(flag, want, m_st, Wpack + oQd, m_d, E);
-  k_bil_mf<TIN, WS><<<E / 16, BS, 0, stream>>>(flag, want, cbf3, m_kt, id3_kt, Wpack + oTc, xt);
-  k_bil_mf<TIN, WS><<<E / 16, BS, 0, stream>>>(flag, want, sbf4, m_d, enb_idx, Wpack + oQc, xq);
-  k_comb2<TIN, WS><<<gE, 512, 0, stream>>>(flag, want, m_st, xt, xq, idx_sw,
-      Wpack + oSk, Wpack + oTst, Wpack + oTts, Wpack + oQst, Wpack + oQts, X, E);
-  k_resE2<TIN, WS><<<gE, 512, 0, stream>>>(flag, want, X, m_st, Wpack + oB0, Wpack + oB1,
-      Wpack + oA0, Wpack + oA1, Wpack + oA2, Wpack + oA3, R2, E);
-  k_zero<<<(N * 128 + BS - 1) / BS, BS, 0, stream>>>(h2, N * 128);
-  k_scatter<TIN><<<E, 128, 0, stream>>>(flag, want, R2, rbf_h, W_ae_rbf, idx_t, h2);
-  k_gemmN2<WS><<<gN, 512, 0, stream>>>(flag, want, h2, Wpack + oAed, Rn2, N);
-  k_resN2<WS><<<gN, 512, 0, stream>>>(flag, want, Rn2, Wpack + oAe0, Wpack + oAe1,
-                                      Wpack + oAe2, Wpack + oAe3, N);
-  TOUT* out_h = (TOUT*)d_out;
-  TOUT* out_m = out_h + (size_t)N * 128;
-  k_hnew_b<TIN, TOUT><<<(N * 128 + BS - 1) / BS, BS, 0, stream>>>(flag, want, h, Rn2, out_h,
-                                                                  N * 128);
-  k_asi2<TIN, TOUT, WS><<<gE, 512, 0, stream>>>(flag, want, Rn2, R2, idx_s, idx_t,
-      Wpack + oAsi, Wpack + oM0, Wpack + oM1, out_m, E);
+  if (ws) ((float*)out)[i] = v;
+  else    ((bf16_t*)out)[i] = (bf16_t)v;
 }
 
 extern "C" void kernel_launch(void* const* d_in, const int* in_sizes, int n_in,
@@ -833,8 +705,79 @@
 
   k_detect<<<1, 64, 0, stream>>>((const unsigned short*)d_in[2], flag);
 
-  run_pipeline<bf16_t, bf16_t, false>(d_in, N, E, d_out, Wpack, s0, s1, s2, s3, h2, Rn2, flag, 0,
-                                      stream);
-  run_pipeline<float, float, true>(d_in, N, E, d_out, Wpack, s0, s1, s2, s3, h2, Rn2, flag, 1,
-                                   stream);
-}
+  struct Def { int idx; int Krows; int K, Np, Kpad, bilin; };
+  const Def defs[25] = {
+      {23, 0, 128, 64, 128, 0},
+      {17, 0, 128, 128, 128, 0},
+      {18, 0, 16, 128, 32, 0},
+      {19, 0, 128, 64, 128, 0},
+      {21, 0, 64, 128, 64, 0},
+      {22, 0, 64, 128, 64, 0},
+      {25, 0, 64, 128, 64, 0},
+      {26, 0, 64, 128, 64, 0},
+      {16, 0, 128, 128, 128, 0},
+      {27, 0, 128, 128, 128, 0},
+      {27, 128, 128, 128, 128, 0},
+      {28, 0, 128, 128, 128, 0},
+      {28, 128, 128, 128, 128, 0},
+      {28, 256, 128, 128, 128, 0},
+      {28, 384, 128, 128, 128, 0},
+      {29, 0, 128, 128, 128, 0},
+      {29, 128, 128, 128, 128, 0},
+      {31, 0, 128, 128, 128, 0},
+      {32, 0, 128, 128, 128, 0},
+      {32, 128, 128, 128, 128, 0},
+      {32, 256, 128, 128, 128, 0},
+      {32, 384, 128, 128, 128, 0},
+      {33, 0, 384, 128, 384, 0},
+      {20, 0, 1024, 64, 1024, 1},
+      {24, 0, 1024, 64, 1024, 1},
+  };
+  RTable tab;
+  int off[25];
+  int cur = 0;
+  for (int i = 0; i < 25; ++i) {
+    off[i] = cur;
+    tab.d[i].src = d_in[defs[i].idx];
+    tab.d[i].K = defs[i].K;
+    tab.d[i].N = defs[i].Np;
+    tab.d[i].Kpad = defs[i].Kpad;
+    tab.d[i].dstoff = cur;
+    tab.d[i].mode = (defs[i].Krows << 1) | defs[i].bilin;
+    cur += 2 * defs[i].Kpad * defs[i].Np;
+  }
+
+  k_repack<<<dim3(256, 25), 256, 0, stream>>>(flag, tab, Wpack);
+
+  bf16_t* mkt_tmp = s0;
+  bf16_t* m_kt = s2;
+  bf16_t* m_d  = s3;
+  bf16_t* xt = s0;
+  bf16_t* xq = s1;
+  bf16_t* X  = s2;
+  bf16_t* R2 = s0;
+
+  const int gE64 = E / 64;
+  const int gN64 = N / 64;
+
+  k_mkt2<<<gE64, 256, 0, stream>>>(flag, d_in[1], d_in[3], Wpack + off[1], Wpack + off[2],
+                                   mkt_tmp);
+  k_gemmE2<<<gE64, 256, 0, stream>>>(flag, 0, mkt_tmp, Wpack + off[3], m_kt);
+  k_gemmE2<<<gE64, 256, 0, stream>>>(flag, 1, d_in[1], Wpack + off[0], m_d);
+  k_bil<<<E / 16, 256, 0, stream>>>(flag, d_in[4], m_kt, (const int*)d_in[9], Wpack + off[23],
+                                    xt);
+  k_bil<<<E / 16, 256, 0, stream>>>(flag, d_in[5], m_d, (const int*)d_in[12], Wpack + off[24],
+                                    xq);
+  k_comb2<<<gE64, 256, 0, stream>>>(flag, d_in[1], xt, xq, (const int*)d_in[8],
+      Wpack + off[8], Wpack + off[4], Wpack + off[5], Wpack + off[6], Wpack + off[7], X);
+  k_resE2<<<gE64, 256, 0, stream>>>(flag, X, d_in[1], Wpack + off[9], Wpack + off[10],
+      Wpack + off[11], Wpack + off[12], Wpack + off[13], Wpack + off[14], R2);
+  k_zero<<<(N * 128 + 255) / 256, 256, 0, stream>>>(h2, N * 128);
+  k_scatter<<<E, 128, 0, stream>>>(flag, R2, d_in[2], d_in[30], (const int*)d_in[7], h2);
+  k_gemmN2<<<gN64, 256, 0, stream>>>(flag, h2, Wpack + off[17], Rn2);
+  k_resN2<<<gN64, 256, 0, stream>>>(flag, Rn2, Wpack + off[18], Wpack + off[19],
+                                    Wpack + off[20], Wpack + off[21]);
+  k_hnew<<<(N * 128 + 255) / 256, 256, 0, stream>>>(flag, d_in[0], Rn2, d_out, N * 128);
+  k_asi2<<<gE64, 256, 0, stream>>>(flag, Rn2, R2, (const int*)d_in[6], (const int*)d_in[7],
+      Wpack + off[22], Wpack + off[15], Wpack + off[16], d_out, N * 128);
+}
```
